# Kernel optimization log

Measured on AMD Instinct MI355X. Metric: run time of the kernel, lower is better.

Reference implementation:

```python
import jax, jax.numpy as jnp
import numpy as np

N = 50000      # nodes
E = 800000     # edges
IN = 128       # in_dim
EMB = 32       # emb_dim
ED = 8         # edge_dim
L = 4          # num_layers
B = 64         # num graphs in batch
OUT = 10       # out_dim
EPS = 1e-5


def setup_inputs() -> dict:
    key = jax.random.key(0)
    ks = jax.random.split(key, 16)
    f32 = jnp.float32
    def nrm(k, shape, scale):
        return jax.random.normal(k, shape, dtype=f32) * scale
    inp = {}
    inp['x'] = nrm(ks[0], (N, IN), 1.0)
    inp['edge_index'] = jax.random.randint(ks[1], (2, E), 0, N)
    inp['edge_attr'] = nrm(ks[2], (E, ED), 1.0)
    inp['batch'] = jnp.sort(jax.random.randint(ks[3], (N,), 0, B))
    # lin_in
    inp['lin_in_w'] = nrm(ks[4], (IN, EMB), 0.05)
    inp['lin_in_b'] = jnp.zeros((EMB,), f32)
    # per-layer message MLP: Linear(2e+ed->e), BN, ReLU, Linear(e->e), BN, ReLU
    inp['msg_w1'] = nrm(ks[5], (L, 2 * EMB + ED, EMB), 0.1)
    inp['msg_b1'] = jnp.zeros((L, EMB), f32)
    inp['msg_g1'] = jnp.ones((L, EMB), f32)
    inp['msg_be1'] = jnp.zeros((L, EMB), f32)
    inp['msg_w2'] = nrm(ks[6], (L, EMB, EMB), 0.1)
    inp['msg_b2'] = jnp.zeros((L, EMB), f32)
    inp['msg_g2'] = jnp.ones((L, EMB), f32)
    inp['msg_be2'] = jnp.zeros((L, EMB), f32)
    # per-layer update MLP: Linear(2e->e), BN, ReLU, Linear(e->e), BN, ReLU
    inp['upd_w1'] = nrm(ks[7], (L, 2 * EMB, EMB), 0.1)
    inp['upd_b1'] = jnp.zeros((L, EMB), f32)
    inp['upd_g1'] = jnp.ones((L, EMB), f32)
    inp['upd_be1'] = jnp.zeros((L, EMB), f32)
    inp['upd_w2'] = nrm(ks[8], (L, EMB, EMB), 0.1)
    inp['upd_b2'] = jnp.zeros((L, EMB), f32)
    inp['upd_g2'] = jnp.ones((L, EMB), f32)
    inp['upd_be2'] = jnp.zeros((L, EMB), f32)
    # lin_pred
    inp['pred_w'] = nrm(ks[9], (EMB, OUT), 0.1)
    inp['pred_b'] = jnp.zeros((OUT,), f32)
    return inp


def _bn(x, g, b):
    # BatchNorm1d in training mode: batch stats over dim 0 (biased variance)
    mu = jnp.mean(x, axis=0)
    var = jnp.mean(jnp.square(x - mu), axis=0)
    return (x - mu) * jax.lax.rsqrt(var + EPS) * g + b


def reference(x, edge_attr, lin_in_w, lin_in_b,
              msg_w1, msg_b1, msg_g1, msg_be1, msg_w2, msg_b2, msg_g2, msg_be2,
              upd_w1, upd_b1, upd_g1, upd_be1, upd_w2, upd_b2, upd_g2, upd_be2,
              pred_w, pred_b, edge_index, batch):
    src = edge_index[0]  # h_j source nodes
    dst = edge_index[1]  # h_i target nodes (aggregation index)
    h = x @ lin_in_w + lin_in_b  # [N, EMB]
    for i in range(L):
        # message: gather + concat + MLP(BN,ReLU)x2 over edges
        msg_in = jnp.concatenate([h[dst], h[src], edge_attr], axis=-1)  # [E, 2e+ed]
        m = jax.nn.relu(_bn(msg_in @ msg_w1[i] + msg_b1[i], msg_g1[i], msg_be1[i]))
        m = jax.nn.relu(_bn(m @ msg_w2[i] + msg_b2[i], msg_g2[i], msg_be2[i]))
        # aggregate: scatter-add by destination
        aggr = jax.ops.segment_sum(m, dst, num_segments=N)  # [N, EMB]
        # update: concat + MLP(BN,ReLU)x2
        u = jnp.concatenate([h, aggr], axis=-1)  # [N, 2e]
        u = jax.nn.relu(_bn(u @ upd_w1[i] + upd_b1[i], upd_g1[i], upd_be1[i]))
        u = jax.nn.relu(_bn(u @ upd_w2[i] + upd_b2[i], upd_g2[i], upd_be2[i]))
        h = u + h  # residual in MPNNModel.get_embeddings
    # global mean pool
    sums = jax.ops.segment_sum(h, batch, num_segments=B)
    counts = jax.ops.segment_sum(jnp.ones((N,), h.dtype), batch, num_segments=B)
    h_graph = sums / jnp.maximum(counts, 1.0)[:, None]
    return h_graph @ pred_w + pred_b  # [B, OUT]
```

## Files before the change

### kernel.cpp

```cpp
#include <hip/hip_runtime.h>
#include <cstddef>

#define N_NODES 50000
#define N_EDGES 800000
#define IN_DIM  128
#define EMB     32
#define ED      8
#define NLAYERS 4
#define NB      64
#define OUTD    10
#define EPS_BN  1e-5f

#define EDGE_GRID 3125
#define NODE_GRID 196
#define NODE4_GRID 782
#define AGGR_GRID 6250
#define MSG1_EPT  2
#define MSG1_GRID 1563
#define NT16      50000
#define MSG2_TPW  16
#define MSG2_GRID 782

#define SREP 4

typedef short bf16x8 __attribute__((ext_vector_type(8)));
typedef float f32x4  __attribute__((ext_vector_type(4)));


__device__ __forceinline__ unsigned short f2bf(float x) {
  union { float f; unsigned u; } v; v.f = x;
  unsigned b = v.u + 0x7FFFu + ((v.u >> 16) & 1u);
  return (unsigned short)(b >> 16);
}
__device__ __forceinline__ float bf2f(unsigned short s) {
  union { unsigned u; float f; } v; v.u = ((unsigned)s) << 16;
  return v.f;
}

__device__ __forceinline__ uint4 pack8_bf16(const float v[8]) {
  uint4 o;
  o.x = (unsigned)f2bf(v[0]) | ((unsigned)f2bf(v[1]) << 16);
  o.y = (unsigned)f2bf(v[2]) | ((unsigned)f2bf(v[3]) << 16);
  o.z = (unsigned)f2bf(v[4]) | ((unsigned)f2bf(v[5]) << 16);
  o.w = (unsigned)f2bf(v[6]) | ((unsigned)f2bf(v[7]) << 16);
  return o;
}

__device__ __forceinline__ void mac8_f4(float acc[8], const float4 v, const float* __restrict__ wk) {
#pragma unroll
  for (int j = 0; j < 8; ++j) acc[j] = fmaf(v.x, wk[j], acc[j]);
#pragma unroll
  for (int j = 0; j < 8; ++j) acc[j] = fmaf(v.y, wk[EMB + j], acc[j]);
#pragma unroll
  for (int j = 0; j < 8; ++j) acc[j] = fmaf(v.z, wk[2*EMB + j], acc[j]);
#pragma unroll
  for (int j = 0; j < 8; ++j) acc[j] = fmaf(v.w, wk[3*EMB + j], acc[j]);
}

__device__ __forceinline__ void coef_from_stats(const float* __restrict__ stats_stage,
                                                const float* __restrict__ g,
                                                const float* __restrict__ be,
                                                float inv_count, float* __restrict__ cf) {
  if (threadIdx.x < EMB) {
    const int c = threadIdx.x;
    float s = 0.f, ss = 0.f;
#pragma unroll
    for (int r = 0; r < SREP; ++r) {
      s  += stats_stage[r*64 + c];
      ss += stats_stage[r*64 + EMB + c];
    }
    const float mu  = s * inv_count;
    const float var = ss * inv_count - mu*mu;
    const float a = g[c] * rsqrtf(var + EPS_BN);
    cf[c] = a;
    cf[EMB + c] = fmaf(-mu, a, be[c]);
  }
  __syncthreads();
}

__device__ __forceinline__ void wave_stats_atomic(float ts[8], float tss[8],
                                                  float* __restrict__ lds_s,
                                                  float* __restrict__ lds_q,
                                                  float* __restrict__ stats_stage) {
  const int lane = threadIdx.x & 63;
  const int wv   = threadIdx.x >> 6;
#pragma unroll
  for (int j = 0; j < 8; ++j) {
    float a = ts[j], b = tss[j];
#pragma unroll
    for (int o = 32; o > 0; o >>= 1) {
      a += __shfl_down(a, o, 64);
      b += __shfl_down(b, o, 64);
    }
    ts[j] = a; tss[j] = b;
  }
  if (lane == 0) {
#pragma unroll
    for (int j = 0; j < 8; ++j) {
      lds_s[wv*8 + j] = ts[j];
      lds_q[wv*8 + j] = tss[j];
    }
  }
  __syncthreads();
  if (threadIdx.x < 64) {
    const float v = (threadIdx.x < 32) ? lds_s[threadIdx.x] : lds_q[threadIdx.x - 32];
    atomicAdd(stats_stage + ((blockIdx.x & (SREP-1)) << 6) + threadIdx.x, v);
  }
}

__device__ __forceinline__ void block_stats_atomic(const float ts[EMB], const float tss[EMB],
                                                   float* __restrict__ stats_stage) {
  __shared__ float sred[256];
  const int lane = threadIdx.x & 63;
  const int wid  = threadIdx.x >> 6;
#pragma unroll
  for (int c = 0; c < EMB; ++c) {
    float a = ts[c];
    float q = tss[c];
#pragma unroll
    for (int o = 32; o > 0; o >>= 1) {
      a += __shfl_down(a, o, 64);
      q += __shfl_down(q, o, 64);
    }
    if (lane == 0) { sred[wid*64 + c] = a; sred[wid*64 + EMB + c] = q; }
  }
  __syncthreads();
  if (threadIdx.x < 64) {
    const float v = sred[threadIdx.x] + sred[64 + threadIdx.x] +
                    sred[128 + threadIdx.x] + sred[192 + threadIdx.x];
    atomicAdd(stats_stage + ((blockIdx.x & (SREP-1)) << 6) + threadIdx.x, v);
  }
}


__global__ __launch_bounds__(256) void k_lin_in_pq(
    const float* __restrict__ x, const float* __restrict__ w, const float* __restrict__ b,
    const float* __restrict__ w1, const float* __restrict__ b1,
    float* __restrict__ h, unsigned short* __restrict__ p, unsigned short* __restrict__ q)
{
  __shared__ float lds_h[64][33];
  const int lane = threadIdx.x & 63;
  const int wv   = threadIdx.x >> 6;
  const int n  = blockIdx.x*64 + lane;
  const int c0 = wv*8;
  if (n < N_NODES) {
    float acc[8];
#pragma unroll
    for (int j = 0; j < 8; ++j) acc[j] = b[c0 + j];
    const float4* xp = (const float4*)(x + (size_t)n*IN_DIM);
#pragma unroll 8
    for (int k4 = 0; k4 < IN_DIM/4; ++k4)
      mac8_f4(acc, xp[k4], w + (k4*4)*EMB + c0);
    float4 o0, o1;
    o0.x = acc[0]; o0.y = acc[1]; o0.z = acc[2]; o0.w = acc[3];
    o1.x = acc[4]; o1.y = acc[5]; o1.z = acc[6]; o1.w = acc[7];
    *(float4*)(h + (size_t)n*EMB + c0)     = o0;
    *(float4*)(h + (size_t)n*EMB + c0 + 4) = o1;
#pragma unroll
    for (int j = 0; j < 8; ++j) lds_h[lane][c0 + j] = acc[j];
  }
  __syncthreads();
  if (n < N_NODES) {
    float ap[8], aq[8];
#pragma unroll
    for (int j = 0; j < 8; ++j) { ap[j] = b1[c0 + j]; aq[j] = 0.f; }
#pragma unroll
    for (int k = 0; k < EMB; ++k) {
      const float hv = lds_h[lane][k];
      const float* wp = w1 + k*EMB + c0;
      const float* wq = w1 + (EMB + k)*EMB + c0;
#pragma unroll
      for (int j = 0; j < 8; ++j) ap[j] = fmaf(hv, wp[j], ap[j]);
#pragma unroll
      for (int j = 0; j < 8; ++j) aq[j] = fmaf(hv, wq[j], aq[j]);
    }
    *(uint4*)(p + (size_t)n*EMB + c0) = pack8_bf16(ap);
    *(uint4*)(q + (size_t)n*EMB + c0) = pack8_bf16(aq);
  }
}

__global__ __launch_bounds__(256) void k_upd1(
    const float* __restrict__ h, float* __restrict__ aggr,
    const float* __restrict__ w, const float* __restrict__ b,
    float* __restrict__ stats)
{
  __shared__ float lds_s[32], lds_q[32];
  const int lane = threadIdx.x & 63;
  const int wv   = threadIdx.x >> 6;
  const int n  = blockIdx.x*64 + lane;
  const int c0 = wv*8;
  float acc[8];
#pragma unroll
  for (int j = 0; j < 8; ++j) acc[j] = 0.f;
  if (n < N_NODES) {
#pragma unroll
    for (int j = 0; j < 8; ++j) acc[j] = b[c0 + j];
    const float4* hp = (const float4*)(h + (size_t)n*EMB);
    const float4* ap = (const float4*)(aggr + (size_t)n*EMB);
#pragma unroll
    for (int k4 = 0; k4 < 8; ++k4) mac8_f4(acc, hp[k4], w + (k4*4)*EMB + c0);
#pragma unroll
    for (int k4 = 0; k4 < 8; ++k4) mac8_f4(acc, ap[k4], w + (EMB + k4*4)*EMB + c0);
  }
  float ts[8], tss[8];
#pragma unroll
  for (int j = 0; j < 8; ++j) { ts[j] = acc[j]; tss[j] = acc[j]*acc[j]; }
  wave_stats_atomic(ts, tss, lds_s, lds_q, stats);
  if (n < N_NODES) {
    float4 o0, o1;
    o0.x = acc[0]; o0.y = acc[1]; o0.z = acc[2]; o0.w = acc[3];
    o1.x = acc[4]; o1.y = acc[5]; o1.z = acc[6]; o1.w = acc[7];
    *(float4*)(aggr + (size_t)n*EMB + c0)     = o0;
    *(float4*)(aggr + (size_t)n*EMB + c0 + 4) = o1;
  }
}

__global__ __launch_bounds__(256) void k_upd2(
    float* __restrict__ z,
    const float* __restrict__ stats1, const float* __restrict__ g1, const float* __restrict__ be1,
    const float* __restrict__ w, const float* __restrict__ b,
    float* __restrict__ stats2)
{
  __shared__ float cf[64];
  __shared__ float lds_s[32], lds_q[32];
  coef_from_stats(stats1, g1, be1, 1.0f/(float)N_NODES, cf);

  const int lane = threadIdx.x & 63;
  const int wv   = threadIdx.x >> 6;
  const int n  = blockIdx.x*64 + lane;
  const int c0 = wv*8;
  float acc[8];
#pragma unroll
  for (int j = 0; j < 8; ++j) acc[j] = 0.f;
  if (n < N_NODES) {
#pragma unroll
    for (int j = 0; j < 8; ++j) acc[j] = b[c0 + j];
    const float4* zp = (const float4*)(z + (size_t)n*EMB);
#pragma unroll
    for (int k4 = 0; k4 < 8; ++k4) {
      const float4 v = zp[k4];
      const float mv[4] = {v.x, v.y, v.z, v.w};
#pragma unroll
      for (int t = 0; t < 4; ++t) {
        const int k = 4*k4 + t;
        const float m = fmaxf(fmaf(cf[k], mv[t], cf[EMB + k]), 0.f);
        const float* wk = w + k*EMB + c0;
#pragma unroll
        for (int j = 0; j < 8; ++j) acc[j] = fmaf(m, wk[j], acc[j]);
      }
    }
  }
  float ts[8], tss[8];
#pragma unroll
  for (int j = 0; j < 8; ++j) { ts[j] = acc[j]; tss[j] = acc[j]*acc[j]; }
  wave_stats_atomic(ts, tss, lds_s, lds_q, stats2);
  if (n < N_NODES) {
    float4 o0, o1;
    o0.x = acc[0]; o0.y = acc[1]; o0.z = acc[2]; o0.w = acc[3];
    o1.x = acc[4]; o1.y = acc[5]; o1.z = acc[6]; o1.w = acc[7];
    *(float4*)(z + (size_t)n*EMB + c0)     = o0;
    *(float4*)(z + (size_t)n*EMB + c0 + 4) = o1;
  }
}

__global__ __launch_bounds__(256) void k_resid_pq(
    float* __restrict__ h, const float* __restrict__ z,
    const float* __restrict__ stats, const float* __restrict__ g, const float* __restrict__ be,
    const float* __restrict__ w1_next, const float* __restrict__ b1_next,
    unsigned short* __restrict__ p, unsigned short* __restrict__ q)
{
  __shared__ float cf[64];
  __shared__ float lds_h[64][33];
  coef_from_stats(stats, g, be, 1.0f/(float)N_NODES, cf);

  const int lane = threadIdx.x & 63;
  const int wv   = threadIdx.x >> 6;
  const int n  = blockIdx.x*64 + lane;
  const int c0 = wv*8;
  if (n < N_NODES) {
    const float4* zp = (const float4*)(z + (size_t)n*EMB + c0);
    float4* hp = (float4*)(h + (size_t)n*EMB + c0);
    float hn[8];
    const float4 z0 = zp[0], z1 = zp[1];
    const float4 h0 = hp[0], h1 = hp[1];
    const float zv[8] = {z0.x, z0.y, z0.z, z0.w, z1.x, z1.y, z1.z, z1.w};
    const float hv[8] = {h0.x, h0.y, h0.z, h0.w, h1.x, h1.y, h1.z, h1.w};
#pragma unroll
    for (int j = 0; j < 8; ++j) {
      const int k = c0 + j;
      hn[j] = hv[j] + fmaxf(fmaf(cf[k], zv[j], cf[EMB + k]), 0.f);
      lds_h[lane][k] = hn[j];
    }
    float4 o0, o1;
    o0.x = hn[0]; o0.y = hn[1]; o0.z = hn[2]; o0.w = hn[3];
    o1.x = hn[4]; o1.y = hn[5]; o1.z = hn[6]; o1.w = hn[7];
    hp[0] = o0; hp[1] = o1;
  }
  __syncthreads();
  if (n < N_NODES && w1_next) {
    float ap[8], aq[8];
#pragma unroll
    for (int j = 0; j < 8; ++j) { ap[j] = b1_next[c0 + j]; aq[j] = 0.f; }
#pragma unroll
    for (int k = 0; k < EMB; ++k) {
      const float hvv = lds_h[lane][k];
      const float* wp = w1_next + k*EMB + c0;
      const float* wq = w1_next + (EMB + k)*EMB + c0;
#pragma unroll
      for (int j = 0; j < 8; ++j) ap[j] = fmaf(hvv, wp[j], ap[j]);
#pragma unroll
      for (int j = 0; j < 8; ++j) aq[j] = fmaf(hvv, wq[j], aq[j]);
    }
    *(uint4*)(p + (size_t)n*EMB + c0) = pack8_bf16(ap);
    *(uint4*)(q + (size_t)n*EMB + c0) = pack8_bf16(aq);
  }
}

__global__ __launch_bounds__(256) void k_hist(const int* __restrict__ ei, int* __restrict__ cnt) {
  const int e = blockIdx.x*256 + threadIdx.x;
  if (e < N_EDGES) atomicAdd(&cnt[ei[N_EDGES + e]], 1);
}

__global__ __launch_bounds__(256) void k_scan_a(const int* __restrict__ cnt,
                                                int* __restrict__ row_ptr, int* __restrict__ bsum) {
  __shared__ int s[256];
  const int gid = blockIdx.x*256 + threadIdx.x;
  const int v = (gid < N_NODES) ? cnt[gid] : 0;
  s[threadIdx.x] = v;
  __syncthreads();
  for (int o = 1; o < 256; o <<= 1) {
    const int t = (threadIdx.x >= o) ? s[threadIdx.x - o] : 0;
    __syncthreads();
    s[threadIdx.x] += t;
    __syncthreads();
  }
  if (gid < N_NODES) row_ptr[gid] = s[threadIdx.x] - v;
  if (threadIdx.x == 255) bsum[blockIdx.x] = s[255];
}

__global__ __launch_bounds__(256) void k_scan_b(int* __restrict__ bsum, int* __restrict__ row_ptr) {
  __shared__ int s[256];
  const int v = (threadIdx.x < NODE_GRID) ? bsum[threadIdx.x] : 0;
  s[threadIdx.x] = v;
  __syncthreads();
  for (int o = 1; o < 256; o <<= 1) {
    const int t = (threadIdx.x >= o) ? s[threadIdx.x - o] : 0;
    __syncthreads();
    s[threadIdx.x] += t;
    __syncthreads();
  }
  if (threadIdx.x < NODE_GRID) bsum[threadIdx.x] = s[threadIdx.x] - v;
  if (threadIdx.x == 0) row_ptr[N_NODES] = N_EDGES;
}

__global__ __launch_bounds__(256) void k_scan_c(int* __restrict__ row_ptr, const int* __restrict__ bsum) {
  const int gid = blockIdx.x*256 + threadIdx.x;
  if (gid < N_NODES) row_ptr[gid] += bsum[blockIdx.x];
}

__global__ __launch_bounds__(256) void k_place(const int* __restrict__ ei,
                                               const int* __restrict__ row_ptr,
                                               int* __restrict__ cnt2, int* __restrict__ perm) {
  const int e = blockIdx.x*256 + threadIdx.x;
  if (e >= N_EDGES) return;
  const int d = ei[N_EDGES + e];
  const int pos = row_ptr[d] + atomicAdd(&cnt2[d], 1);
  perm[pos] = e;
}

__global__ __launch_bounds__(256) void k_permute(
    const int* __restrict__ perm, const int* __restrict__ ei, const float* __restrict__ ea,
    int* __restrict__ src_perm, int* __restrict__ dst_perm, unsigned short* __restrict__ ea_perm)
{
  const int i = blockIdx.x*256 + threadIdx.x;
  const int e = perm[i];
  src_perm[i] = ei[e];
  dst_perm[i] = ei[N_EDGES + e];
  const float4* src4 = (const float4*)(ea + (size_t)e*ED);
  const float4 v0 = src4[0], v1 = src4[1];
  const float ev[8] = {v0.x, v0.y, v0.z, v0.w, v1.x, v1.y, v1.z, v1.w};
  unsigned u[4];
#pragma unroll
  for (int j = 0; j < 4; ++j)
    u[j] = (unsigned)f2bf(ev[2*j]) | ((unsigned)f2bf(ev[2*j+1]) << 16);
  uint4 o; o.x = u[0]; o.y = u[1]; o.z = u[2]; o.w = u[3];
  *(uint4*)(ea_perm + (size_t)i*ED) = o;
}


__global__ __launch_bounds__(256) void k_msg1(
    const unsigned short* __restrict__ pb, const unsigned short* __restrict__ qb,
    const int* __restrict__ src_perm, const int* __restrict__ dst_perm,
    const unsigned short* __restrict__ ea_perm,
    const float* __restrict__ w1b,
    unsigned short* __restrict__ y, float* __restrict__ stats)
{
  float ts[EMB], tss[EMB];
#pragma unroll
  for (int c = 0; c < EMB; ++c) { ts[c] = 0.f; tss[c] = 0.f; }
  const int base = blockIdx.x*(256*MSG1_EPT) + threadIdx.x;
  for (int it = 0; it < MSG1_EPT; ++it) {
    const int i = base + it*256;
    if (i >= N_EDGES) break;
    const int dst = dst_perm[i];
    const int src = src_perm[i];
    float acc[EMB];
    const uint4* pd = (const uint4*)(pb + (size_t)dst*EMB);
    const uint4* qs = (const uint4*)(qb + (size_t)src*EMB);
#pragma unroll
    for (int j4 = 0; j4 < 4; ++j4) {
      const uint4 a = pd[j4];
      const uint4 b = qs[j4];
      const unsigned ua[4] = {a.x, a.y, a.z, a.w};
      const unsigned ub[4] = {b.x, b.y, b.z, b.w};
#pragma unroll
      for (int t = 0; t < 4; ++t) {
        acc[j4*8 + 2*t]   = bf2f((unsigned short)(ua[t] & 0xFFFFu)) +
                            bf2f((unsigned short)(ub[t] & 0xFFFFu));
        acc[j4*8 + 2*t+1] = bf2f((unsigned short)(ua[t] >> 16)) +
                            bf2f((unsigned short)(ub[t] >> 16));
      }
    }
    const uint4 eraw = *(const uint4*)(ea_perm + (size_t)i*ED);
    const unsigned ue[4] = {eraw.x, eraw.y, eraw.z, eraw.w};
    float ev[8];
#pragma unroll
    for (int t = 0; t < 4; ++t) {
      ev[2*t]   = bf2f((unsigned short)(ue[t] & 0xFFFFu));
      ev[2*t+1] = bf2f((unsigned short)(ue[t] >> 16));
    }
#pragma unroll
    for (int k = 0; k < 8; ++k) {
      const float* wk = w1b + k*EMB;
#pragma unroll
      for (int c = 0; c < EMB; ++c) acc[c] = fmaf(ev[k], wk[c], acc[c]);
    }

    unsigned short us[EMB];
#pragma unroll
    for (int c = 0; c < EMB; ++c) us[c] = f2bf(acc[c]);
    unsigned u[16];
#pragma unroll
    for (int j = 0; j < 16; ++j)
      u[j] = (unsigned)us[2*j] | ((unsigned)us[2*j+1] << 16);
    uint4* dp = (uint4*)(y + (size_t)i*EMB);
#pragma unroll
    for (int j = 0; j < 4; ++j) {
      uint4 o; o.x = u[4*j]; o.y = u[4*j+1]; o.z = u[4*j+2]; o.w = u[4*j+3];
      dp[j] = o;
    }
#pragma unroll
    for (int c = 0; c < EMB; ++c) {
      const float v = bf2f(us[c]);
      ts[c] += v;
      tss[c] = fmaf(v, v, tss[c]);
    }
  }
  block_stats_atomic(ts, tss, stats);
}

__global__ __launch_bounds__(256) void k_msg2(
    unsigned short* __restrict__ y,
    const float* __restrict__ stats1, const float* __restrict__ g1, const float* __restrict__ be1,
    const float* __restrict__ w2, const float* __restrict__ b2,
    float* __restrict__ stats2)
{
  __shared__ __align__(16) unsigned short lds_t[4][16*32];
  __shared__ float lds_s[4][32], lds_q[4][32];
  __shared__ float cf[64];

  coef_from_stats(stats1, g1, be1, 1.0f/(float)N_EDGES, cf);

  const int lane = threadIdx.x & 63;
  const int wid  = threadIdx.x >> 6;
  const int n0 = lane & 15;
  const int kb = lane >> 4;

  bf16x8 Blo, Bhi;
#pragma unroll
  for (int j = 0; j < 8; ++j) {
    Blo[j] = (short)f2bf(w2[(kb*8 + j)*EMB + n0]);
    Bhi[j] = (short)f2bf(w2[(kb*8 + j)*EMB + 16 + n0]);
  }
  float a1[8], c1[8];
#pragma unroll
  for (int j = 0; j < 8; ++j) {
    a1[j] = cf[kb*8 + j];
    c1[j] = cf[EMB + kb*8 + j];
  }
  const float b2c0 = b2[n0], b2c1 = b2[16 + n0];

  float ts[8], tss[8];
#pragma unroll
  for (int j = 0; j < 8; ++j) { ts[j] = 0.f; tss[j] = 0.f; }

  const int tile0 = blockIdx.x * (MSG2_TPW*4);
  for (int t = 0; t < MSG2_TPW; ++t) {
    const int tile = tile0 + t*4 + wid;
    if (tile >= NT16) break;
    const size_t e0 = (size_t)tile * 16;

    const uint4 araw = *(const uint4*)(y + (e0 + n0)*EMB + kb*8);
    unsigned int ua[4] = {araw.x, araw.y, araw.z, araw.w};
    bf16x8 A;
#pragma unroll
    for (int j = 0; j < 4; ++j) {
      float v0 = bf2f((unsigned short)(ua[j] & 0xFFFFu));
      float v1 = bf2f((unsigned short)(ua[j] >> 16));
      v0 = fmaxf(fmaf(a1[2*j],   v0, c1[2*j]),   0.f);
      v1 = fmaxf(fmaf(a1[2*j+1], v1, c1[2*j+1]), 0.f);
      A[2*j]   = (short)f2bf(v0);
      A[2*j+1] = (short)f2bf(v1);
    }

    f32x4 acc0 = {0.f, 0.f, 0.f, 0.f};
    f32x4 acc1 = {0.f, 0.f, 0.f, 0.f};
    acc0 = __builtin_amdgcn_mfma_f32_16x16x32_bf16(A, Blo, acc0, 0, 0, 0);
    acc1 = __builtin_amdgcn_mfma_f32_16x16x32_bf16(A, Bhi, acc1, 0, 0, 0);

#pragma unroll
    for (int r = 0; r < 4; ++r) {
      const int row = kb*4 + r;
      lds_t[wid][row*32 + n0]      = f2bf(acc0[r] + b2c0);
      lds_t[wid][row*32 + 16 + n0] = f2bf(acc1[r] + b2c1);
    }
    const uint4 orow = *(const uint4*)&lds_t[wid][(lane>>2)*32 + (lane&3)*8];
    *(uint4*)(y + (e0 + (lane>>2))*EMB + (lane&3)*8) = orow;

    unsigned int uo[4] = {orow.x, orow.y, orow.z, orow.w};
#pragma unroll
    for (int j = 0; j < 4; ++j) {
      const float v0 = bf2f((unsigned short)(uo[j] & 0xFFFFu));
      const float v1 = bf2f((unsigned short)(uo[j] >> 16));
      ts[2*j]   += v0;  tss[2*j]   = fmaf(v0, v0, tss[2*j]);
      ts[2*j+1] += v1;  tss[2*j+1] = fmaf(v1, v1, tss[2*j+1]);
    }
  }

#pragma unroll
  for (int j = 0; j < 8; ++j) {
    float s = ts[j], qq = tss[j];
#pragma unroll
    for (int o = 4; o < 64; o <<= 1) {
      s  += __shfl_xor(s, o, 64);
      qq += __shfl_xor(qq, o, 64);
    }
    ts[j] = s; tss[j] = qq;
  }
  if (lane < 4) {
#pragma unroll
    for (int j = 0; j < 8; ++j) {
      lds_s[wid][lane*8 + j] = ts[j];
      lds_q[wid][lane*8 + j] = tss[j];
    }
  }
  __syncthreads();
  if (threadIdx.x < 64) {
    const int c = threadIdx.x & 31;
    const int kind = threadIdx.x >> 5;
    float v = 0.f;
#pragma unroll
    for (int wq = 0; wq < 4; ++wq)
      v += kind ? lds_q[wq][c] : lds_s[wq][c];
    atomicAdd(stats2 + ((blockIdx.x & (SREP-1)) << 6) + kind*32 + c, v);
  }
}

__global__ __launch_bounds__(256) void k_aggr(
    const unsigned short* __restrict__ y, const int* __restrict__ row_ptr,
    const float* __restrict__ stats2, const float* __restrict__ g2, const float* __restrict__ be2,
    float* __restrict__ aggr)
{
  __shared__ float cf[64];
  coef_from_stats(stats2, g2, be2, 1.0f/(float)N_EDGES, cf);

  const int grp = threadIdx.x >> 5;
  const int l   = threadIdx.x & 31;
  const int rof = l >> 4;
  const int cp  = l & 15;
  const int n = blockIdx.x*8 + grp;
  if (n >= N_NODES) return;
  const float a0 = cf[2*cp],     b0 = cf[EMB + 2*cp];
  const float a1 = cf[2*cp + 1], b1 = cf[EMB + 2*cp + 1];
  const int lo = row_ptr[n], hi = row_ptr[n+1];
  float s0 = 0.f, s1 = 0.f;
  for (int i = lo + rof; i < hi; i += 2) {
    const unsigned u = *(const unsigned*)(y + (size_t)i*EMB + 2*cp);
    const float v0 = bf2f((unsigned short)(u & 0xFFFFu));
    const float v1 = bf2f((unsigned short)(u >> 16));
    s0 += fmaxf(fmaf(a0, v0, b0), 0.f);
    s1 += fmaxf(fmaf(a1, v1, b1), 0.f);
  }
  s0 += __shfl_xor(s0, 16, 64);
  s1 += __shfl_xor(s1, 16, 64);
  if (rof == 0) {
    float2 o; o.x = s0; o.y = s1;
    *(float2*)(aggr + (size_t)n*EMB + 2*cp) = o;
  }
}

__global__ void k_pool(const float* __restrict__ h, const int* __restrict__ batch,
                       const float* __restrict__ pw, const float* __restrict__ pb,
                       float* __restrict__ out)
{
  __shared__ float sred[256];
  __shared__ float hg[EMB];
  const int b = blockIdx.x;
  int lo = 0, hi = N_NODES;
  while (lo < hi) { int m = (lo + hi) >> 1; if (batch[m] < b) lo = m + 1; else hi = m; }
  const int start = lo;
  hi = N_NODES;
  while (lo < hi) { int m = (lo + hi) >> 1; if (batch[m] < b + 1) lo = m + 1; else hi = m; }
  const int end = lo;

  const int c = threadIdx.x & (EMB-1);
  const int r = threadIdx.x >> 5;
  float s = 0.f;
  for (int n = start + r; n < end; n += 8) s += h[(size_t)n*EMB + c];
  sred[threadIdx.x] = s;
  __syncthreads();
  if (threadIdx.x < EMB) {
    float tot = 0.f;
#pragma unroll
    for (int r2 = 0; r2 < 8; ++r2) tot += sred[r2*EMB + threadIdx.x];
    const float cnt = (float)(end - start);
    hg[threadIdx.x] = tot / fmaxf(cnt, 1.f);
  }
  __syncthreads();
  if (threadIdx.x < OUTD) {
    float acc = pb[threadIdx.x];
#pragma unroll
    for (int cc = 0; cc < EMB; ++cc) acc = fmaf(hg[cc], pw[cc*OUTD + threadIdx.x], acc);
    out[b*OUTD + threadIdx.x] = acc;
  }
}


extern "C" void kernel_launch(void* const* d_in, const int* in_sizes, int n_in,
                              void* d_out, int out_size, void* d_ws, size_t ws_size,
                              hipStream_t stream) {
  const float* x        = (const float*)d_in[0];
  const int*   ei       = (const int*)  d_in[1];
  const float* ea       = (const float*)d_in[2];
  const int*   batch    = (const int*)  d_in[3];
  const float* lin_in_w = (const float*)d_in[4];
  const float* lin_in_b = (const float*)d_in[5];
  const float* msg_w1   = (const float*)d_in[6];
  const float* msg_b1   = (const float*)d_in[7];
  const float* msg_g1   = (const float*)d_in[8];
  const float* msg_be1  = (const float*)d_in[9];
  const float* msg_w2   = (const float*)d_in[10];
  const float* msg_b2   = (const float*)d_in[11];
  const float* msg_g2   = (const float*)d_in[12];
  const float* msg_be2  = (const float*)d_in[13];
  const float* upd_w1   = (const float*)d_in[14];
  const float* upd_b1   = (const float*)d_in[15];
  const float* upd_g1   = (const float*)d_in[16];
  const float* upd_be1  = (const float*)d_in[17];
  const float* upd_w2   = (const float*)d_in[18];
  const float* upd_b2   = (const float*)d_in[19];
  const float* upd_g2   = (const float*)d_in[20];
  const float* upd_be2  = (const float*)d_in[21];
  const float* pred_w   = (const float*)d_in[22];
  const float* pred_b   = (const float*)d_in[23];
  float* out = (float*)d_out;

  char* wsb = (char*)d_ws;
  unsigned short* y  = (unsigned short*)wsb;
  unsigned short* eap= (unsigned short*)(wsb + (size_t)N_EDGES*EMB*2);
  unsigned short* p  = eap + (size_t)N_EDGES*ED;
  unsigned short* q  = p + (size_t)N_NODES*EMB;
  float* h       = (float*)(q + (size_t)N_NODES*EMB);
  float* aggr    = h + (size_t)N_NODES*EMB;
  float* stats   = aggr + (size_t)N_NODES*EMB;
  int*   cnt     = (int*)(stats + 16*SREP*64);
  int*   cnt2    = cnt + N_NODES;
  int*   row_ptr = cnt2 + N_NODES;
  int*   bsum    = row_ptr + N_NODES + 1;
  int*   perm    = bsum + 256;
  int*   src_perm= perm + N_EDGES;
  int*   dst_perm= src_perm + N_EDGES;
  const size_t need = ((size_t)((char*)(dst_perm + N_EDGES) - wsb));
  if (ws_size < need) return;

  hipMemsetAsync(stats, 0, (16*SREP*64 + 2*N_NODES)*sizeof(float), stream);

  k_lin_in_pq<<<NODE4_GRID, 256, 0, stream>>>(x, lin_in_w, lin_in_b, msg_w1, msg_b1, h, p, q);
  k_hist<<<EDGE_GRID, 256, 0, stream>>>(ei, cnt);
  k_scan_a<<<NODE_GRID, 256, 0, stream>>>(cnt, row_ptr, bsum);
  k_scan_b<<<1, 256, 0, stream>>>(bsum, row_ptr);
  k_scan_c<<<NODE_GRID, 256, 0, stream>>>(row_ptr, bsum);
  k_place<<<EDGE_GRID, 256, 0, stream>>>(ei, row_ptr, cnt2, perm);
  k_permute<<<EDGE_GRID, 256, 0, stream>>>(perm, ei, ea, src_perm, dst_perm, eap);

  for (int l = 0; l < NLAYERS; ++l) {
    const int st = l*4;
    const float* w1  = msg_w1 + (size_t)l*(2*EMB+ED)*EMB;
    const float* w1b = w1 + (size_t)2*EMB*EMB;
    const float* w2  = msg_w2 + (size_t)l*EMB*EMB;
    const float* uw1 = upd_w1 + (size_t)l*(2*EMB)*EMB;
    const float* uw2 = upd_w2 + (size_t)l*EMB*EMB;
    const float* w1_next = (l+1 < NLAYERS) ? msg_w1 + (size_t)(l+1)*(2*EMB+ED)*EMB : nullptr;
    const float* b1_next = (l+1 < NLAYERS) ? msg_b1 + (size_t)(l+1)*EMB : nullptr;

    k_msg1<<<MSG1_GRID, 256, 0, stream>>>(p, q, src_perm, dst_perm, eap,
                                          w1b, y, stats + (size_t)st*SREP*64);
    k_msg2<<<MSG2_GRID, 256, 0, stream>>>(y, stats + (size_t)st*SREP*64,
                                          msg_g1 + l*EMB, msg_be1 + l*EMB,
                                          w2, msg_b2 + l*EMB, stats + (size_t)(st+1)*SREP*64);
    k_aggr<<<AGGR_GRID, 256, 0, stream>>>(y, row_ptr, stats + (size_t)(st+1)*SREP*64,
                                          msg_g2 + l*EMB, msg_be2 + l*EMB, aggr);
    k_upd1<<<NODE4_GRID, 256, 0, stream>>>(h, aggr, uw1, upd_b1 + l*EMB,
                                           stats + (size_t)(st+2)*SREP*64);
    k_upd2<<<NODE4_GRID, 256, 0, stream>>>(aggr, stats + (size_t)(st+2)*SREP*64,
                                           upd_g1 + l*EMB, upd_be1 + l*EMB,
                                           uw2, upd_b2 + l*EMB, stats + (size_t)(st+3)*SREP*64);
    k_resid_pq<<<NODE4_GRID, 256, 0, stream>>>(h, aggr, stats + (size_t)(st+3)*SREP*64,
                                               upd_g2 + l*EMB, upd_be2 + l*EMB,
                                               w1_next, b1_next, p, q);
  }

  k_pool<<<NB, 256, 0, stream>>>(h, batch, pred_w, pred_b, out);
}
```

Before: 951.7 us.

## Fuse all GNN stages into one persistent cooperative kernel with grid syncs

Replaces about thirty separate kernel launches (preprocessing, four layers of six stages each, and pooling) with a single cooperative persistent kernel that loops over work with grid-stride loops and separates dependent stages with grid.sync(). The goal is to remove per-launch overhead and the gaps between dependent kernels. In exchange the grid is capped at occupancy × 256 CUs (at most 1024 blocks), register pressure rises from merging every stage into one kernel, and each stage now pays a grid-wide barrier. A new z buffer is added to the workspace.

```diff
diff --git a/kernel.cpp b/kernel.cpp
--- a/kernel.cpp
+++ b/kernel.cpp
@@ -1,5 +1,8 @@
 #include <hip/hip_runtime.h>
+#include <hip/hip_cooperative_groups.h>
 #include <cstddef>
+
+namespace cg = cooperative_groups;
 
 #define N_NODES 50000
 #define N_EDGES 800000
@@ -11,16 +14,8 @@
 #define OUTD    10
 #define EPS_BN  1e-5f
 
-#define EDGE_GRID 3125
 #define NODE_GRID 196
-#define NODE4_GRID 782
-#define AGGR_GRID 6250
-#define MSG1_EPT  2
-#define MSG1_GRID 1563
 #define NT16      50000
-#define MSG2_TPW  16
-#define MSG2_GRID 782
-
 #define SREP 4
 
 typedef short bf16x8 __attribute__((ext_vector_type(8)));
@@ -46,7 +41,7 @@
   return o;
 }
 
-__device__ __forceinline__ void mac8_f4(float acc[8], const float4 v, const float* __restrict__ wk) {
+__device__ __forceinline__ void mac8_f4(float acc[8], const float4 v, const float* wk) {
 #pragma unroll
   for (int j = 0; j < 8; ++j) acc[j] = fmaf(v.x, wk[j], acc[j]);
 #pragma unroll
@@ -57,581 +52,583 @@
   for (int j = 0; j < 8; ++j) acc[j] = fmaf(v.w, wk[3*EMB + j], acc[j]);
 }
 
-__device__ __forceinline__ void coef_from_stats(const float* __restrict__ stats_stage,
-                                                const float* __restrict__ g,
-                                                const float* __restrict__ be,
-                                                float inv_count, float* __restrict__ cf) {
-  if (threadIdx.x < EMB) {
-    const int c = threadIdx.x;
-    float s = 0.f, ss = 0.f;
-#pragma unroll
-    for (int r = 0; r < SREP; ++r) {
-      s  += stats_stage[r*64 + c];
-      ss += stats_stage[r*64 + EMB + c];
-    }
-    const float mu  = s * inv_count;
-    const float var = ss * inv_count - mu*mu;
-    const float a = g[c] * rsqrtf(var + EPS_BN);
-    cf[c] = a;
-    cf[EMB + c] = fmaf(-mu, a, be[c]);
+struct KArgs {
+  const float* x; const int* ei; const float* ea; const int* batch;
+  const float *lin_in_w, *lin_in_b;
+  const float *msg_w1, *msg_b1, *msg_g1, *msg_be1;
+  const float *msg_w2, *msg_b2, *msg_g2, *msg_be2;
+  const float *upd_w1, *upd_b1, *upd_g1, *upd_be1;
+  const float *upd_w2, *upd_b2, *upd_g2, *upd_be2;
+  const float *pred_w, *pred_b;
+  unsigned short *y, *eap, *p, *q;
+  float *h, *aggr, *z, *stats;
+  int *cnt, *cnt2, *row_ptr, *bsum, *perm, *src_perm, *dst_perm;
+  float* out;
+};
+
+
+__global__ __launch_bounds__(256, 4) void k_all(KArgs a)
+{
+  cg::grid_group grid = cg::this_grid();
+  const int tid  = threadIdx.x;
+  const int lane = tid & 63;
+  const int wv   = tid >> 6;
+  const int nblk = gridDim.x;
+
+  __shared__ float lds_h[64][33];
+  __shared__ __align__(16) unsigned short lds_t[4][512];
+  __shared__ float lds_s4[4][32], lds_q4[4][32];
+  __shared__ float lds_ws_s[32], lds_ws_q[32];
+  __shared__ float sred[256];
+  __shared__ float cf[64];
+  __shared__ int   sscan[256];
+  __shared__ float hg[EMB];
+
+  const float invE = 1.0f / (float)N_EDGES;
+  const float invN = 1.0f / (float)N_NODES;
+
+  for (int n0 = blockIdx.x*64; n0 < N_NODES; n0 += nblk*64) {
+    const int n  = n0 + lane;
+    const int c0 = wv*8;
+    if (n < N_NODES) {
+      float acc[8];
+#pragma unroll
+      for (int j = 0; j < 8; ++j) acc[j] = a.lin_in_b[c0 + j];
+      const float4* xp = (const float4*)(a.x + (size_t)n*IN_DIM);
+#pragma unroll 8
+      for (int k4 = 0; k4 < IN_DIM/4; ++k4)
+        mac8_f4(acc, xp[k4], a.lin_in_w + (k4*4)*EMB + c0);
+      float4 o0, o1;
+      o0.x = acc[0]; o0.y = acc[1]; o0.z = acc[2]; o0.w = acc[3];
+      o1.x = acc[4]; o1.y = acc[5]; o1.z = acc[6]; o1.w = acc[7];
+      *(float4*)(a.h + (size_t)n*EMB + c0)     = o0;
+      *(float4*)(a.h + (size_t)n*EMB + c0 + 4) = o1;
+#pragma unroll
+      for (int j = 0; j < 8; ++j) lds_h[lane][c0 + j] = acc[j];
+    }
+    __syncthreads();
+    if (n < N_NODES) {
+      float ap[8], aq[8];
+#pragma unroll
+      for (int j = 0; j < 8; ++j) { ap[j] = a.msg_b1[c0 + j]; aq[j] = 0.f; }
+#pragma unroll
+      for (int k = 0; k < EMB; ++k) {
+        const float hv = lds_h[lane][k];
+        const float* wp = a.msg_w1 + k*EMB + c0;
+        const float* wq = a.msg_w1 + (EMB + k)*EMB + c0;
+#pragma unroll
+        for (int j = 0; j < 8; ++j) ap[j] = fmaf(hv, wp[j], ap[j]);
+#pragma unroll
+        for (int j = 0; j < 8; ++j) aq[j] = fmaf(hv, wq[j], aq[j]);
+      }
+      *(uint4*)(a.p + (size_t)n*EMB + c0) = pack8_bf16(ap);
+      *(uint4*)(a.q + (size_t)n*EMB + c0) = pack8_bf16(aq);
+    }
+    __syncthreads();
   }
-  __syncthreads();
-}
-
-__device__ __forceinline__ void wave_stats_atomic(float ts[8], float tss[8],
-                                                  float* __restrict__ lds_s,
-                                                  float* __restrict__ lds_q,
-                                                  float* __restrict__ stats_stage) {
-  const int lane = threadIdx.x & 63;
-  const int wv   = threadIdx.x >> 6;
-#pragma unroll
-  for (int j = 0; j < 8; ++j) {
-    float a = ts[j], b = tss[j];
-#pragma unroll
-    for (int o = 32; o > 0; o >>= 1) {
-      a += __shfl_down(a, o, 64);
-      b += __shfl_down(b, o, 64);
-    }
-    ts[j] = a; tss[j] = b;
+  for (int e = blockIdx.x*256 + tid; e < N_EDGES; e += nblk*256)
+    atomicAdd(&a.cnt[a.ei[N_EDGES + e]], 1);
+  grid.sync();
+
+  for (int blk = blockIdx.x; blk < NODE_GRID; blk += nblk) {
+    const int gid = blk*256 + tid;
+    const int v = (gid < N_NODES) ? a.cnt[gid] : 0;
+    sscan[tid] = v;
+    __syncthreads();
+    for (int o = 1; o < 256; o <<= 1) {
+      const int t = (tid >= o) ? sscan[tid - o] : 0;
+      __syncthreads();
+      sscan[tid] += t;
+      __syncthreads();
+    }
+    if (gid < N_NODES) a.row_ptr[gid] = sscan[tid] - v;
+    if (tid == 255) a.bsum[blk] = sscan[255];
+    __syncthreads();
   }
-  if (lane == 0) {
-#pragma unroll
-    for (int j = 0; j < 8; ++j) {
-      lds_s[wv*8 + j] = ts[j];
-      lds_q[wv*8 + j] = tss[j];
-    }
+  grid.sync();
+
+  if (blockIdx.x == 0) {
+    const int v = (tid < NODE_GRID) ? a.bsum[tid] : 0;
+    sscan[tid] = v;
+    __syncthreads();
+    for (int o = 1; o < 256; o <<= 1) {
+      const int t = (tid >= o) ? sscan[tid - o] : 0;
+      __syncthreads();
+      sscan[tid] += t;
+      __syncthreads();
+    }
+    if (tid < NODE_GRID) a.bsum[tid] = sscan[tid] - v;
+    if (tid == 0) a.row_ptr[N_NODES] = N_EDGES;
   }
-  __syncthreads();
-  if (threadIdx.x < 64) {
-    const float v = (threadIdx.x < 32) ? lds_s[threadIdx.x] : lds_q[threadIdx.x - 32];
-    atomicAdd(stats_stage + ((blockIdx.x & (SREP-1)) << 6) + threadIdx.x, v);
+  grid.sync();
+
+  for (int gid = blockIdx.x*256 + tid; gid < N_NODES; gid += nblk*256)
+    a.row_ptr[gid] += a.bsum[gid >> 8];
+  grid.sync();
+
+  for (int e = blockIdx.x*256 + tid; e < N_EDGES; e += nblk*256) {
+    const int d = a.ei[N_EDGES + e];
+    const int pos = a.row_ptr[d] + atomicAdd(&a.cnt2[d], 1);
+    a.perm[pos] = e;
   }
-}
-
-__device__ __forceinline__ void block_stats_atomic(const float ts[EMB], const float tss[EMB],
-                                                   float* __restrict__ stats_stage) {
-  __shared__ float sred[256];
-  const int lane = threadIdx.x & 63;
-  const int wid  = threadIdx.x >> 6;
-#pragma unroll
-  for (int c = 0; c < EMB; ++c) {
-    float a = ts[c];
-    float q = tss[c];
-#pragma unroll
-    for (int o = 32; o > 0; o >>= 1) {
-      a += __shfl_down(a, o, 64);
-      q += __shfl_down(q, o, 64);
-    }
-    if (lane == 0) { sred[wid*64 + c] = a; sred[wid*64 + EMB + c] = q; }
+  grid.sync();
+
+  for (int i = blockIdx.x*256 + tid; i < N_EDGES; i += nblk*256) {
+    const int e = a.perm[i];
+    a.src_perm[i] = a.ei[e];
+    a.dst_perm[i] = a.ei[N_EDGES + e];
+    const float4* src4 = (const float4*)(a.ea + (size_t)e*ED);
+    const float4 v0 = src4[0], v1 = src4[1];
+    const float ev[8] = {v0.x, v0.y, v0.z, v0.w, v1.x, v1.y, v1.z, v1.w};
+    unsigned u[4];
+#pragma unroll
+    for (int j = 0; j < 4; ++j)
+      u[j] = (unsigned)f2bf(ev[2*j]) | ((unsigned)f2bf(ev[2*j+1]) << 16);
+    uint4 o; o.x = u[0]; o.y = u[1]; o.z = u[2]; o.w = u[3];
+    *(uint4*)(a.eap + (size_t)i*ED) = o;
   }
-  __syncthreads();
-  if (threadIdx.x < 64) {
-    const float v = sred[threadIdx.x] + sred[64 + threadIdx.x] +
-                    sred[128 + threadIdx.x] + sred[192 + threadIdx.x];
-    atomicAdd(stats_stage + ((blockIdx.x & (SREP-1)) << 6) + threadIdx.x, v);
+  grid.sync();
+
+  for (int l = 0; l < NLAYERS; ++l) {
+    const int st = l*4;
+    const float* w1b = a.msg_w1 + (size_t)l*(2*EMB+ED)*EMB + (size_t)2*EMB*EMB;
+    const float* w2  = a.msg_w2 + (size_t)l*EMB*EMB;
+    const float* uw1 = a.upd_w1 + (size_t)l*(2*EMB)*EMB;
+    const float* uw2 = a.upd_w2 + (size_t)l*EMB*EMB;
+    float* st0 = a.stats + (size_t)st*SREP*64;
+    float* st1 = a.stats + (size_t)(st+1)*SREP*64;
+    float* st2 = a.stats + (size_t)(st+2)*SREP*64;
+    float* st3 = a.stats + (size_t)(st+3)*SREP*64;
+
+    {
+      float ts[EMB], tss[EMB];
+#pragma unroll
+      for (int c = 0; c < EMB; ++c) { ts[c] = 0.f; tss[c] = 0.f; }
+      for (int i = blockIdx.x*256 + tid; i < N_EDGES; i += nblk*256) {
+        const int dst = a.dst_perm[i];
+        const int src = a.src_perm[i];
+        float acc[EMB];
+        const uint4* pd = (const uint4*)(a.p + (size_t)dst*EMB);
+        const uint4* qs = (const uint4*)(a.q + (size_t)src*EMB);
+#pragma unroll
+        for (int j4 = 0; j4 < 4; ++j4) {
+          const uint4 av = pd[j4];
+          const uint4 bv = qs[j4];
+          const unsigned ua[4] = {av.x, av.y, av.z, av.w};
+          const unsigned ub[4] = {bv.x, bv.y, bv.z, bv.w};
+#pragma unroll
+          for (int t = 0; t < 4; ++t) {
+            acc[j4*8 + 2*t]   = bf2f((unsigned short)(ua[t] & 0xFFFFu)) +
+                                bf2f((unsigned short)(ub[t] & 0xFFFFu));
+            acc[j4*8 + 2*t+1] = bf2f((unsigned short)(ua[t] >> 16)) +
+                                bf2f((unsigned short)(ub[t] >> 16));
+          }
+        }
+        const uint4 eraw = *(const uint4*)(a.eap + (size_t)i*ED);
+        const unsigned ue[4] = {eraw.x, eraw.y, eraw.z, eraw.w};
+        float ev[8];
+#pragma unroll
+        for (int t = 0; t < 4; ++t) {
+          ev[2*t]   = bf2f((unsigned short)(ue[t] & 0xFFFFu));
+          ev[2*t+1] = bf2f((unsigned short)(ue[t] >> 16));
+        }
+#pragma unroll
+        for (int k = 0; k < 8; ++k) {
+          const float* wk = w1b + k*EMB;
+#pragma unroll
+          for (int c = 0; c < EMB; ++c) acc[c] = fmaf(ev[k], wk[c], acc[c]);
+        }
+        unsigned short us[EMB];
+#pragma unroll
+        for (int c = 0; c < EMB; ++c) us[c] = f2bf(acc[c]);
+        unsigned u[16];
+#pragma unroll
+        for (int j = 0; j < 16; ++j)
+          u[j] = (unsigned)us[2*j] | ((unsigned)us[2*j+1] << 16);
+        uint4* dp = (uint4*)(a.y + (size_t)i*EMB);
+#pragma unroll
+        for (int j = 0; j < 4; ++j) {
+          uint4 o; o.x = u[4*j]; o.y = u[4*j+1]; o.z = u[4*j+2]; o.w = u[4*j+3];
+          dp[j] = o;
+        }
+#pragma unroll
+        for (int c = 0; c < EMB; ++c) {
+          const float v = bf2f(us[c]);
+          ts[c] += v;
+          tss[c] = fmaf(v, v, tss[c]);
+        }
+      }
+#pragma unroll
+      for (int c = 0; c < EMB; ++c) {
+        float aa = ts[c];
+        float qq = tss[c];
+#pragma unroll
+        for (int o = 32; o > 0; o >>= 1) {
+          aa += __shfl_down(aa, o, 64);
+          qq += __shfl_down(qq, o, 64);
+        }
+        if (lane == 0) { sred[wv*64 + c] = aa; sred[wv*64 + EMB + c] = qq; }
+      }
+      __syncthreads();
+      if (tid < 64) {
+        const float v = sred[tid] + sred[64 + tid] + sred[128 + tid] + sred[192 + tid];
+        atomicAdd(st0 + ((blockIdx.x & (SREP-1)) << 6) + tid, v);
+      }
+      __syncthreads();
+    }
+    grid.sync();
+
+    {
+      if (tid < EMB) {
+        float s = 0.f, ss = 0.f;
+#pragma unroll
+        for (int r = 0; r < SREP; ++r) { s += st0[r*64 + tid]; ss += st0[r*64 + EMB + tid]; }
+        const float mu  = s * invE;
+        const float var = ss * invE - mu*mu;
+        const float aa = a.msg_g1[l*EMB + tid] * rsqrtf(var + EPS_BN);
+        cf[tid] = aa;
+        cf[EMB + tid] = fmaf(-mu, aa, a.msg_be1[l*EMB + tid]);
+      }
+      __syncthreads();
+
+      const int n0i = lane & 15;
+      const int kb  = lane >> 4;
+      bf16x8 Blo, Bhi;
+#pragma unroll
+      for (int j = 0; j < 8; ++j) {
+        Blo[j] = (short)f2bf(w2[(kb*8 + j)*EMB + n0i]);
+        Bhi[j] = (short)f2bf(w2[(kb*8 + j)*EMB + 16 + n0i]);
+      }
+      float a1[8], c1[8];
+#pragma unroll
+      for (int j = 0; j < 8; ++j) {
+        a1[j] = cf[kb*8 + j];
+        c1[j] = cf[EMB + kb*8 + j];
+      }
+      const float b2c0 = a.msg_b2[l*EMB + n0i], b2c1 = a.msg_b2[l*EMB + 16 + n0i];
+
+      float ts8[8], tss8[8];
+#pragma unroll
+      for (int j = 0; j < 8; ++j) { ts8[j] = 0.f; tss8[j] = 0.f; }
+
+      for (int tile = blockIdx.x*4 + wv; tile < NT16; tile += nblk*4) {
+        const size_t e0 = (size_t)tile * 16;
+        const uint4 araw = *(const uint4*)(a.y + (e0 + n0i)*EMB + kb*8);
+        unsigned int ua[4] = {araw.x, araw.y, araw.z, araw.w};
+        bf16x8 A;
+#pragma unroll
+        for (int j = 0; j < 4; ++j) {
+          float v0 = bf2f((unsigned short)(ua[j] & 0xFFFFu));
+          float v1 = bf2f((unsigned short)(ua[j] >> 16));
+          v0 = fmaxf(fmaf(a1[2*j],   v0, c1[2*j]),   0.f);
+          v1 = fmaxf(fmaf(a1[2*j+1], v1, c1[2*j+1]), 0.f);
+          A[2*j]   = (short)f2bf(v0);
+          A[2*j+1] = (short)f2bf(v1);
+        }
+        f32x4 acc0 = {0.f, 0.f, 0.f, 0.f};
+        f32x4 acc1 = {0.f, 0.f, 0.f, 0.f};
+        acc0 = __builtin_amdgcn_mfma_f32_16x16x32_bf16(A, Blo, acc0, 0, 0, 0);
+        acc1 = __builtin_amdgcn_mfma_f32_16x16x32_bf16(A, Bhi, acc1, 0, 0, 0);
+#pragma unroll
+        for (int r = 0; r < 4; ++r) {
+          const int row = kb*4 + r;
+          lds_t[wv][row*32 + n0i]      = f2bf(acc0[r] + b2c0);
+          lds_t[wv][row*32 + 16 + n0i] = f2bf(acc1[r] + b2c1);
+        }
+        const uint4 orow = *(const uint4*)&lds_t[wv][(lane>>2)*32 + (lane&3)*8];
+        *(uint4*)(a.y + (e0 + (lane>>2))*EMB + (lane&3)*8) = orow;
+        unsigned int uo[4] = {orow.x, orow.y, orow.z, orow.w};
+#pragma unroll
+        for (int j = 0; j < 4; ++j) {
+          const float v0 = bf2f((unsigned short)(uo[j] & 0xFFFFu));
+          const float v1 = bf2f((unsigned short)(uo[j] >> 16));
+          ts8[2*j]   += v0;  tss8[2*j]   = fmaf(v0, v0, tss8[2*j]);
+          ts8[2*j+1] += v1;  tss8[2*j+1] = fmaf(v1, v1, tss8[2*j+1]);
+        }
+      }
+#pragma unroll
+      for (int j = 0; j < 8; ++j) {
+        float s = ts8[j], qq = tss8[j];
+#pragma unroll
+        for (int o = 4; o < 64; o <<= 1) {
+          s  += __shfl_xor(s, o, 64);
+          qq += __shfl_xor(qq, o, 64);
+        }
+        ts8[j] = s; tss8[j] = qq;
+      }
+      if (lane < 4) {
+#pragma unroll
+        for (int j = 0; j < 8; ++j) {
+          lds_s4[wv][lane*8 + j] = ts8[j];
+          lds_q4[wv][lane*8 + j] = tss8[j];
+        }
+      }
+      __syncthreads();
+      if (tid < 64) {
+        const int c = tid & 31;
+        const int kind = tid >> 5;
+        float v = 0.f;
+#pragma unroll
+        for (int wq = 0; wq < 4; ++wq)
+          v += kind ? lds_q4[wq][c] : lds_s4[wq][c];
+        atomicAdd(st1 + ((blockIdx.x & (SREP-1)) << 6) + kind*32 + c, v);
+      }
+      __syncthreads();
+    }
+    grid.sync();
+
+    {
+      if (tid < EMB) {
+        float s = 0.f, ss = 0.f;
+#pragma unroll
+        for (int r = 0; r < SREP; ++r) { s += st1[r*64 + tid]; ss += st1[r*64 + EMB + tid]; }
+        const float mu  = s * invE;
+        const float var = ss * invE - mu*mu;
+        const float aa = a.msg_g2[l*EMB + tid] * rsqrtf(var + EPS_BN);
+        cf[tid] = aa;
+        cf[EMB + tid] = fmaf(-mu, aa, a.msg_be2[l*EMB + tid]);
+      }
+      __syncthreads();
+
+      const int grp = tid >> 5;
+      const int ll  = tid & 31;
+      const int rof = ll >> 4;
+      const int cp  = ll & 15;
+      const float a0 = cf[2*cp],     b0 = cf[EMB + 2*cp];
+      const float a1c = cf[2*cp + 1], b1c = cf[EMB + 2*cp + 1];
+      for (int n = blockIdx.x*8 + grp; n < N_NODES; n += nblk*8) {
+        const int lo = a.row_ptr[n], hi = a.row_ptr[n+1];
+        float s0 = 0.f, s1 = 0.f;
+        for (int i = lo + rof; i < hi; i += 2) {
+          const unsigned u = *(const unsigned*)(a.y + (size_t)i*EMB + 2*cp);
+          const float v0 = bf2f((unsigned short)(u & 0xFFFFu));
+          const float v1 = bf2f((unsigned short)(u >> 16));
+          s0 += fmaxf(fmaf(a0, v0, b0), 0.f);
+          s1 += fmaxf(fmaf(a1c, v1, b1c), 0.f);
+        }
+        s0 += __shfl_xor(s0, 16, 64);
+        s1 += __shfl_xor(s1, 16, 64);
+        if (rof == 0) {
+          float2 o; o.x = s0; o.y = s1;
+          *(float2*)(a.aggr + (size_t)n*EMB + 2*cp) = o;
+        }
+      }
+      __syncthreads();
+    }
+    grid.sync();
+
+    {
+      const int c0 = wv*8;
+      float ts8[8], tss8[8];
+#pragma unroll
+      for (int j = 0; j < 8; ++j) { ts8[j] = 0.f; tss8[j] = 0.f; }
+      for (int nb0 = blockIdx.x*64; nb0 < N_NODES; nb0 += nblk*64) {
+        const int n = nb0 + lane;
+        float acc[8];
+#pragma unroll
+        for (int j = 0; j < 8; ++j) acc[j] = 0.f;
+        if (n < N_NODES) {
+#pragma unroll
+          for (int j = 0; j < 8; ++j) acc[j] = a.upd_b1[l*EMB + c0 + j];
+          const float4* hp = (const float4*)(a.h + (size_t)n*EMB);
+          const float4* ap = (const float4*)(a.aggr + (size_t)n*EMB);
+#pragma unroll
+          for (int k4 = 0; k4 < 8; ++k4) mac8_f4(acc, hp[k4], uw1 + (k4*4)*EMB + c0);
+#pragma unroll
+          for (int k4 = 0; k4 < 8; ++k4) mac8_f4(acc, ap[k4], uw1 + (EMB + k4*4)*EMB + c0);
+          float4 o0, o1;
+          o0.x = acc[0]; o0.y = acc[1]; o0.z = acc[2]; o0.w = acc[3];
+          o1.x = acc[4]; o1.y = acc[5]; o1.z = acc[6]; o1.w = acc[7];
+          *(float4*)(a.z + (size_t)n*EMB + c0)     = o0;
+          *(float4*)(a.z + (size_t)n*EMB + c0 + 4) = o1;
+        }
+#pragma unroll
+        for (int j = 0; j < 8; ++j) { ts8[j] += acc[j]; tss8[j] = fmaf(acc[j], acc[j], tss8[j]); }
+      }
+#pragma unroll
+      for (int j = 0; j < 8; ++j) {
+        float aa = ts8[j], bb = tss8[j];
+#pragma unroll
+        for (int o = 32; o > 0; o >>= 1) {
+          aa += __shfl_down(aa, o, 64);
+          bb += __shfl_down(bb, o, 64);
+        }
+        ts8[j] = aa; tss8[j] = bb;
+      }
+      if (lane == 0) {
+#pragma unroll
+        for (int j = 0; j < 8; ++j) { lds_ws_s[wv*8 + j] = ts8[j]; lds_ws_q[wv*8 + j] = tss8[j]; }
+      }
+      __syncthreads();
+      if (tid < 64) {
+        const float v = (tid < 32) ? lds_ws_s[tid] : lds_ws_q[tid - 32];
+        atomicAdd(st2 + ((blockIdx.x & (SREP-1)) << 6) + tid, v);
+      }
+      __syncthreads();
+    }
+    grid.sync();
+
+    {
+      if (tid < EMB) {
+        float s = 0.f, ss = 0.f;
+#pragma unroll
+        for (int r = 0; r < SREP; ++r) { s += st2[r*64 + tid]; ss += st2[r*64 + EMB + tid]; }
+        const float mu  = s * invN;
+        const float var = ss * invN - mu*mu;
+        const float aa = a.upd_g1[l*EMB + tid] * rsqrtf(var + EPS_BN);
+        cf[tid] = aa;
+        cf[EMB + tid] = fmaf(-mu, aa, a.upd_be1[l*EMB + tid]);
+      }
+      __syncthreads();
+
+      const int c0 = wv*8;
+      float ts8[8], tss8[8];
+#pragma unroll
+      for (int j = 0; j < 8; ++j) { ts8[j] = 0.f; tss8[j] = 0.f; }
+      for (int nb0 = blockIdx.x*64; nb0 < N_NODES; nb0 += nblk*64) {
+        const int n = nb0 + lane;
+        float acc[8];
+#pragma unroll
+        for (int j = 0; j < 8; ++j) acc[j] = 0.f;
+        if (n < N_NODES) {
+#pragma unroll
+          for (int j = 0; j < 8; ++j) acc[j] = a.upd_b2[l*EMB + c0 + j];
+          const float4* zp = (const float4*)(a.z + (size_t)n*EMB);
+#pragma unroll
+          for (int k4 = 0; k4 < 8; ++k4) {
+            const float4 v = zp[k4];
+            const float mv[4] = {v.x, v.y, v.z, v.w};
+#pragma unroll
+            for (int t = 0; t < 4; ++t) {
+              const int k = 4*k4 + t;
+              const float m = fmaxf(fmaf(cf[k], mv[t], cf[EMB + k]), 0.f);
+              const float* wk = uw2 + k*EMB + c0;
+#pragma unroll
+              for (int j = 0; j < 8; ++j) acc[j] = fmaf(m, wk[j], acc[j]);
+            }
+          }
+          float4 o0, o1;
+          o0.x = acc[0]; o0.y = acc[1]; o0.z = acc[2]; o0.w = acc[3];
+          o1.x = acc[4]; o1.y = acc[5]; o1.z = acc[6]; o1.w = acc[7];
+          *(float4*)(a.aggr + (size_t)n*EMB + c0)     = o0;
+          *(float4*)(a.aggr + (size_t)n*EMB + c0 + 4) = o1;
+        }
+#pragma unroll
+        for (int j = 0; j < 8; ++j) { ts8[j] += acc[j]; tss8[j] = fmaf(acc[j], acc[j], tss8[j]); }
+      }
+#pragma unroll
+      for (int j = 0; j < 8; ++j) {
+        float aa = ts8[j], bb = tss8[j];
+#pragma unroll
+        for (int o = 32; o > 0; o >>= 1) {
+          aa += __shfl_down(aa, o, 64);
+          bb += __shfl_down(bb, o, 64);
+        }
+        ts8[j] = aa; tss8[j] = bb;
+      }
+      if (lane == 0) {
+#pragma unroll
+        for (int j = 0; j < 8; ++j) { lds_ws_s[wv*8 + j] = ts8[j]; lds_ws_q[wv*8 + j] = tss8[j]; }
+      }
+      __syncthreads();
+      if (tid < 64) {
+        const float v = (tid < 32) ? lds_ws_s[tid] : lds_ws_q[tid - 32];
+        atomicAdd(st3 + ((blockIdx.x & (SREP-1)) << 6) + tid, v);
+      }
+      __syncthreads();
+    }
+    grid.sync();
+
+    {
+      if (tid < EMB) {
+        float s = 0.f, ss = 0.f;
+#pragma unroll
+        for (int r = 0; r < SREP; ++r) { s += st3[r*64 + tid]; ss += st3[r*64 + EMB + tid]; }
+        const float mu  = s * invN;
+        const float var = ss * invN - mu*mu;
+        const float aa = a.upd_g2[l*EMB + tid] * rsqrtf(var + EPS_BN);
+        cf[tid] = aa;
+        cf[EMB + tid] = fmaf(-mu, aa, a.upd_be2[l*EMB + tid]);
+      }
+      __syncthreads();
+
+      const float* w1n = (l+1 < NLAYERS) ? a.msg_w1 + (size_t)(l+1)*(2*EMB+ED)*EMB : nullptr;
+      const float* b1n = (l+1 < NLAYERS) ? a.msg_b1 + (size_t)(l+1)*EMB : nullptr;
+      const int c0 = wv*8;
+      for (int nb0 = blockIdx.x*64; nb0 < N_NODES; nb0 += nblk*64) {
+        const int n = nb0 + lane;
+        if (n < N_NODES) {
+          const float4* zp = (const float4*)(a.aggr + (size_t)n*EMB + c0);
+          float4* hp = (float4*)(a.h + (size_t)n*EMB + c0);
+          float hn[8];
+          const float4 z0 = zp[0], z1 = zp[1];
+          const float4 h0 = hp[0], h1 = hp[1];
+          const float zv[8] = {z0.x, z0.y, z0.z, z0.w, z1.x, z1.y, z1.z, z1.w};
+          const float hv[8] = {h0.x, h0.y, h0.z, h0.w, h1.x, h1.y, h1.z, h1.w};
+#pragma unroll
+          for (int j = 0; j < 8; ++j) {
+            const int k = c0 + j;
+            hn[j] = hv[j] + fmaxf(fmaf(cf[k], zv[j], cf[EMB + k]), 0.f);
+            lds_h[lane][k] = hn[j];
+          }
+          float4 o0, o1;
+          o0.x = hn[0]; o0.y = hn[1]; o0.z = hn[2]; o0.w = hn[3];
+          o1.x = hn[4]; o1.y = hn[5]; o1.z = hn[6]; o1.w = hn[7];
+          hp[0] = o0; hp[1] = o1;
+        }
+        __syncthreads();
+        if (n < N_NODES && w1n) {
+          float ap[8], aq[8];
+#pragma unroll
+          for (int j = 0; j < 8; ++j) { ap[j] = b1n[c0 + j]; aq[j] = 0.f; }
+#pragma unroll
+          for (int k = 0; k < EMB; ++k) {
+            const float hvv = lds_h[lane][k];
+            const float* wp = w1n + k*EMB + c0;
+            const float* wq = w1n + (EMB + k)*EMB + c0;
+#pragma unroll
+            for (int j = 0; j < 8; ++j) ap[j] = fmaf(hvv, wp[j], ap[j]);
+#pragma unroll
+            for (int j = 0; j < 8; ++j) aq[j] = fmaf(hvv, wq[j], aq[j]);
+          }
+          *(uint4*)(a.p + (size_t)n*EMB + c0) = pack8_bf16(ap);
+          *(uint4*)(a.q + (size_t)n*EMB + c0) = pack8_bf16(aq);
+        }
+        __syncthreads();
+      }
+    }
+    grid.sync();
   }
-}
-
-
-__global__ __launch_bounds__(256) void k_lin_in_pq(
-    const float* __restrict__ x, const float* __restrict__ w, const float* __restrict__ b,
-    const float* __restrict__ w1, const float* __restrict__ b1,
-    float* __restrict__ h, unsigned short* __restrict__ p, unsigned short* __restrict__ q)
-{
-  __shared__ float lds_h[64][33];
-  const int lane = threadIdx.x & 63;
-  const int wv   = threadIdx.x >> 6;
-  const int n  = blockIdx.x*64 + lane;
-  const int c0 = wv*8;
-  if (n < N_NODES) {
-    float acc[8];
-#pragma unroll
-    for (int j = 0; j < 8; ++j) acc[j] = b[c0 + j];
-    const float4* xp = (const float4*)(x + (size_t)n*IN_DIM);
-#pragma unroll 8
-    for (int k4 = 0; k4 < IN_DIM/4; ++k4)
-      mac8_f4(acc, xp[k4], w + (k4*4)*EMB + c0);
-    float4 o0, o1;
-    o0.x = acc[0]; o0.y = acc[1]; o0.z = acc[2]; o0.w = acc[3];
-    o1.x = acc[4]; o1.y = acc[5]; o1.z = acc[6]; o1.w = acc[7];
-    *(float4*)(h + (size_t)n*EMB + c0)     = o0;
-    *(float4*)(h + (size_t)n*EMB + c0 + 4) = o1;
-#pragma unroll
-    for (int j = 0; j < 8; ++j) lds_h[lane][c0 + j] = acc[j];
-  }
-  __syncthreads();
-  if (n < N_NODES) {
-    float ap[8], aq[8];
-#pragma unroll
-    for (int j = 0; j < 8; ++j) { ap[j] = b1[c0 + j]; aq[j] = 0.f; }
-#pragma unroll
-    for (int k = 0; k < EMB; ++k) {
-      const float hv = lds_h[lane][k];
-      const float* wp = w1 + k*EMB + c0;
-      const float* wq = w1 + (EMB + k)*EMB + c0;
-#pragma unroll
-      for (int j = 0; j < 8; ++j) ap[j] = fmaf(hv, wp[j], ap[j]);
-#pragma unroll
-      for (int j = 0; j < 8; ++j) aq[j] = fmaf(hv, wq[j], aq[j]);
-    }
-    *(uint4*)(p + (size_t)n*EMB + c0) = pack8_bf16(ap);
-    *(uint4*)(q + (size_t)n*EMB + c0) = pack8_bf16(aq);
-  }
-}
-
-__global__ __launch_bounds__(256) void k_upd1(
-    const float* __restrict__ h, float* __restrict__ aggr,
-    const float* __restrict__ w, const float* __restrict__ b,
-    float* __restrict__ stats)
-{
-  __shared__ float lds_s[32], lds_q[32];
-  const int lane = threadIdx.x & 63;
-  const int wv   = threadIdx.x >> 6;
-  const int n  = blockIdx.x*64 + lane;
-  const int c0 = wv*8;
-  float acc[8];
-#pragma unroll
-  for (int j = 0; j < 8; ++j) acc[j] = 0.f;
-  if (n < N_NODES) {
-#pragma unroll
-    for (int j = 0; j < 8; ++j) acc[j] = b[c0 + j];
-    const float4* hp = (const float4*)(h + (size_t)n*EMB);
-    const float4* ap = (const float4*)(aggr + (size_t)n*EMB);
-#pragma unroll
-    for (int k4 = 0; k4 < 8; ++k4) mac8_f4(acc, hp[k4], w + (k4*4)*EMB + c0);
-#pragma unroll
-    for (int k4 = 0; k4 < 8; ++k4) mac8_f4(acc, ap[k4], w + (EMB + k4*4)*EMB + c0);
-  }
-  float ts[8], tss[8];
-#pragma unroll
-  for (int j = 0; j < 8; ++j) { ts[j] = acc[j]; tss[j] = acc[j]*acc[j]; }
-  wave_stats_atomic(ts, tss, lds_s, lds_q, stats);
-  if (n < N_NODES) {
-    float4 o0, o1;
-    o0.x = acc[0]; o0.y = acc[1]; o0.z = acc[2]; o0.w = acc[3];
-    o1.x = acc[4]; o1.y = acc[5]; o1.z = acc[6]; o1.w = acc[7];
-    *(float4*)(aggr + (size_t)n*EMB + c0)     = o0;
-    *(float4*)(aggr + (size_t)n*EMB + c0 + 4) = o1;
-  }
-}
-
-__global__ __launch_bounds__(256) void k_upd2(
-    float* __restrict__ z,
-    const float* __restrict__ stats1, const float* __restrict__ g1, const float* __restrict__ be1,
-    const float* __restrict__ w, const float* __restrict__ b,
-    float* __restrict__ stats2)
-{
-  __shared__ float cf[64];
-  __shared__ float lds_s[32], lds_q[32];
-  coef_from_stats(stats1, g1, be1, 1.0f/(float)N_NODES, cf);
-
-  const int lane = threadIdx.x & 63;
-  const int wv   = threadIdx.x >> 6;
-  const int n  = blockIdx.x*64 + lane;
-  const int c0 = wv*8;
-  float acc[8];
-#pragma unroll
-  for (int j = 0; j < 8; ++j) acc[j] = 0.f;
-  if (n < N_NODES) {
-#pragma unroll
-    for (int j = 0; j < 8; ++j) acc[j] = b[c0 + j];
-    const float4* zp = (const float4*)(z + (size_t)n*EMB);
-#pragma unroll
-    for (int k4 = 0; k4 < 8; ++k4) {
-      const float4 v = zp[k4];
-      const float mv[4] = {v.x, v.y, v.z, v.w};
-#pragma unroll
-      for (int t = 0; t < 4; ++t) {
-        const int k = 4*k4 + t;
-        const float m = fmaxf(fmaf(cf[k], mv[t], cf[EMB + k]), 0.f);
-        const float* wk = w + k*EMB + c0;
-#pragma unroll
-        for (int j = 0; j < 8; ++j) acc[j] = fmaf(m, wk[j], acc[j]);
-      }
-    }
-  }
-  float ts[8], tss[8];
-#pragma unroll
-  for (int j = 0; j < 8; ++j) { ts[j] = acc[j]; tss[j] = acc[j]*acc[j]; }
-  wave_stats_atomic(ts, tss, lds_s, lds_q, stats2);
-  if (n < N_NODES) {
-    float4 o0, o1;
-    o0.x = acc[0]; o0.y = acc[1]; o0.z = acc[2]; o0.w = acc[3];
-    o1.x = acc[4]; o1.y = acc[5]; o1.z = acc[6]; o1.w = acc[7];
-    *(float4*)(z + (size_t)n*EMB + c0)     = o0;
-    *(float4*)(z + (size_t)n*EMB + c0 + 4) = o1;
-  }
-}
-
-__global__ __launch_bounds__(256) void k_resid_pq(
-    float* __restrict__ h, const float* __restrict__ z,
-    const float* __restrict__ stats, const float* __restrict__ g, const float* __restrict__ be,
-    const float* __restrict__ w1_next, const float* __restrict__ b1_next,
-    unsigned short* __restrict__ p, unsigned short* __restrict__ q)
-{
-  __shared__ float cf[64];
-  __shared__ float lds_h[64][33];
-  coef_from_stats(stats, g, be, 1.0f/(float)N_NODES, cf);
-
-  const int lane = threadIdx.x & 63;
-  const int wv   = threadIdx.x >> 6;
-  const int n  = blockIdx.x*64 + lane;
-  const int c0 = wv*8;
-  if (n < N_NODES) {
-    const float4* zp = (const float4*)(z + (size_t)n*EMB + c0);
-    float4* hp = (float4*)(h + (size_t)n*EMB + c0);
-    float hn[8];
-    const float4 z0 = zp[0], z1 = zp[1];
-    const float4 h0 = hp[0], h1 = hp[1];
-    const float zv[8] = {z0.x, z0.y, z0.z, z0.w, z1.x, z1.y, z1.z, z1.w};
-    const float hv[8] = {h0.x, h0.y, h0.z, h0.w, h1.x, h1.y, h1.z, h1.w};
-#pragma unroll
-    for (int j = 0; j < 8; ++j) {
-      const int k = c0 + j;
-      hn[j] = hv[j] + fmaxf(fmaf(cf[k], zv[j], cf[EMB + k]), 0.f);
-      lds_h[lane][k] = hn[j];
-    }
-    float4 o0, o1;
-    o0.x = hn[0]; o0.y = hn[1]; o0.z = hn[2]; o0.w = hn[3];
-    o1.x = hn[4]; o1.y = hn[5]; o1.z = hn[6]; o1.w = hn[7];
-    hp[0] = o0; hp[1] = o1;
-  }
-  __syncthreads();
-  if (n < N_NODES && w1_next) {
-    float ap[8], aq[8];
-#pragma unroll
-    for (int j = 0; j < 8; ++j) { ap[j] = b1_next[c0 + j]; aq[j] = 0.f; }
-#pragma unroll
-    for (int k = 0; k < EMB; ++k) {
-      const float hvv = lds_h[lane][k];
-      const float* wp = w1_next + k*EMB + c0;
-      const float* wq = w1_next + (EMB + k)*EMB + c0;
-#pragma unroll
-      for (int j = 0; j < 8; ++j) ap[j] = fmaf(hvv, wp[j], ap[j]);
-#pragma unroll
-      for (int j = 0; j < 8; ++j) aq[j] = fmaf(hvv, wq[j], aq[j]);
-    }
-    *(uint4*)(p + (size_t)n*EMB + c0) = pack8_bf16(ap);
-    *(uint4*)(q + (size_t)n*EMB + c0) = pack8_bf16(aq);
-  }
-}
-
-__global__ __launch_bounds__(256) void k_hist(const int* __restrict__ ei, int* __restrict__ cnt) {
-  const int e = blockIdx.x*256 + threadIdx.x;
-  if (e < N_EDGES) atomicAdd(&cnt[ei[N_EDGES + e]], 1);
-}
-
-__global__ __launch_bounds__(256) void k_scan_a(const int* __restrict__ cnt,
-                                                int* __restrict__ row_ptr, int* __restrict__ bsum) {
-  __shared__ int s[256];
-  const int gid = blockIdx.x*256 + threadIdx.x;
-  const int v = (gid < N_NODES) ? cnt[gid] : 0;
-  s[threadIdx.x] = v;
-  __syncthreads();
-  for (int o = 1; o < 256; o <<= 1) {
-    const int t = (threadIdx.x >= o) ? s[threadIdx.x - o] : 0;
-    __syncthreads();
-    s[threadIdx.x] += t;
-    __syncthreads();
-  }
-  if (gid < N_NODES) row_ptr[gid] = s[threadIdx.x] - v;
-  if (threadIdx.x == 255) bsum[blockIdx.x] = s[255];
-}
-
-__global__ __launch_bounds__(256) void k_scan_b(int* __restrict__ bsum, int* __restrict__ row_ptr) {
-  __shared__ int s[256];
-  const int v = (threadIdx.x < NODE_GRID) ? bsum[threadIdx.x] : 0;
-  s[threadIdx.x] = v;
-  __syncthreads();
-  for (int o = 1; o < 256; o <<= 1) {
-    const int t = (threadIdx.x >= o) ? s[threadIdx.x - o] : 0;
-    __syncthreads();
-    s[threadIdx.x] += t;
-    __syncthreads();
-  }
-  if (threadIdx.x < NODE_GRID) bsum[threadIdx.x] = s[threadIdx.x] - v;
-  if (threadIdx.x == 0) row_ptr[N_NODES] = N_EDGES;
-}
-
-__global__ __launch_bounds__(256) void k_scan_c(int* __restrict__ row_ptr, const int* __restrict__ bsum) {
-  const int gid = blockIdx.x*256 + threadIdx.x;
-  if (gid < N_NODES) row_ptr[gid] += bsum[blockIdx.x];
-}
-
-__global__ __launch_bounds__(256) void k_place(const int* __restrict__ ei,
-                                               const int* __restrict__ row_ptr,
-                                               int* __restrict__ cnt2, int* __restrict__ perm) {
-  const int e = blockIdx.x*256 + threadIdx.x;
-  if (e >= N_EDGES) return;
-  const int d = ei[N_EDGES + e];
-  const int pos = row_ptr[d] + atomicAdd(&cnt2[d], 1);
-  perm[pos] = e;
-}
-
-__global__ __launch_bounds__(256) void k_permute(
-    const int* __restrict__ perm, const int* __restrict__ ei, const float* __restrict__ ea,
-    int* __restrict__ src_perm, int* __restrict__ dst_perm, unsigned short* __restrict__ ea_perm)
-{
-  const int i = blockIdx.x*256 + threadIdx.x;
-  const int e = perm[i];
-  src_perm[i] = ei[e];
-  dst_perm[i] = ei[N_EDGES + e];
-  const float4* src4 = (const float4*)(ea + (size_t)e*ED);
-  const float4 v0 = src4[0], v1 = src4[1];
-  const float ev[8] = {v0.x, v0.y, v0.z, v0.w, v1.x, v1.y, v1.z, v1.w};
-  unsigned u[4];
-#pragma unroll
-  for (int j = 0; j < 4; ++j)
-    u[j] = (unsigned)f2bf(ev[2*j]) | ((unsigned)f2bf(ev[2*j+1]) << 16);
-  uint4 o; o.x = u[0]; o.y = u[1]; o.z = u[2]; o.w = u[3];
-  *(uint4*)(ea_perm + (size_t)i*ED) = o;
-}
-
-
-__global__ __launch_bounds__(256) void k_msg1(
-    const unsigned short* __restrict__ pb, const unsigned short* __restrict__ qb,
-    const int* __restrict__ src_perm, const int* __restrict__ dst_perm,
-    const unsigned short* __restrict__ ea_perm,
-    const float* __restrict__ w1b,
-    unsigned short* __restrict__ y, float* __restrict__ stats)
-{
-  float ts[EMB], tss[EMB];
-#pragma unroll
-  for (int c = 0; c < EMB; ++c) { ts[c] = 0.f; tss[c] = 0.f; }
-  const int base = blockIdx.x*(256*MSG1_EPT) + threadIdx.x;
-  for (int it = 0; it < MSG1_EPT; ++it) {
-    const int i = base + it*256;
-    if (i >= N_EDGES) break;
-    const int dst = dst_perm[i];
-    const int src = src_perm[i];
-    float acc[EMB];
-    const uint4* pd = (const uint4*)(pb + (size_t)dst*EMB);
-    const uint4* qs = (const uint4*)(qb + (size_t)src*EMB);
-#pragma unroll
-    for (int j4 = 0; j4 < 4; ++j4) {
-      const uint4 a = pd[j4];
-      const uint4 b = qs[j4];
-      const unsigned ua[4] = {a.x, a.y, a.z, a.w};
-      const unsigned ub[4] = {b.x, b.y, b.z, b.w};
-#pragma unroll
-      for (int t = 0; t < 4; ++t) {
-        acc[j4*8 + 2*t]   = bf2f((unsigned short)(ua[t] & 0xFFFFu)) +
-                            bf2f((unsigned short)(ub[t] & 0xFFFFu));
-        acc[j4*8 + 2*t+1] = bf2f((unsigned short)(ua[t] >> 16)) +
-                            bf2f((unsigned short)(ub[t] >> 16));
-      }
-    }
-    const uint4 eraw = *(const uint4*)(ea_perm + (size_t)i*ED);
-    const unsigned ue[4] = {eraw.x, eraw.y, eraw.z, eraw.w};
-    float ev[8];
-#pragma unroll
-    for (int t = 0; t < 4; ++t) {
-      ev[2*t]   = bf2f((unsigned short)(ue[t] & 0xFFFFu));
-      ev[2*t+1] = bf2f((unsigned short)(ue[t] >> 16));
-    }
-#pragma unroll
-    for (int k = 0; k < 8; ++k) {
-      const float* wk = w1b + k*EMB;
-#pragma unroll
-      for (int c = 0; c < EMB; ++c) acc[c] = fmaf(ev[k], wk[c], acc[c]);
-    }
-
-    unsigned short us[EMB];
-#pragma unroll
-    for (int c = 0; c < EMB; ++c) us[c] = f2bf(acc[c]);
-    unsigned u[16];
-#pragma unroll
-    for (int j = 0; j < 16; ++j)
-      u[j] = (unsigned)us[2*j] | ((unsigned)us[2*j+1] << 16);
-    uint4* dp = (uint4*)(y + (size_t)i*EMB);
-#pragma unroll
-    for (int j = 0; j < 4; ++j) {
-      uint4 o; o.x = u[4*j]; o.y = u[4*j+1]; o.z = u[4*j+2]; o.w = u[4*j+3];
-      dp[j] = o;
-    }
-#pragma unroll
-    for (int c = 0; c < EMB; ++c) {
-      const float v = bf2f(us[c]);
-      ts[c] += v;
-      tss[c] = fmaf(v, v, tss[c]);
-    }
-  }
-  block_stats_atomic(ts, tss, stats);
-}
-
-__global__ __launch_bounds__(256) void k_msg2(
-    unsigned short* __restrict__ y,
-    const float* __restrict__ stats1, const float* __restrict__ g1, const float* __restrict__ be1,
-    const float* __restrict__ w2, const float* __restrict__ b2,
-    float* __restrict__ stats2)
-{
-  __shared__ __align__(16) unsigned short lds_t[4][16*32];
-  __shared__ float lds_s[4][32], lds_q[4][32];
-  __shared__ float cf[64];
-
-  coef_from_stats(stats1, g1, be1, 1.0f/(float)N_EDGES, cf);
-
-  const int lane = threadIdx.x & 63;
-  const int wid  = threadIdx.x >> 6;
-  const int n0 = lane & 15;
-  const int kb = lane >> 4;
-
-  bf16x8 Blo, Bhi;
-#pragma unroll
-  for (int j = 0; j < 8; ++j) {
-    Blo[j] = (short)f2bf(w2[(kb*8 + j)*EMB + n0]);
-    Bhi[j] = (short)f2bf(w2[(kb*8 + j)*EMB + 16 + n0]);
-  }
-  float a1[8], c1[8];
-#pragma unroll
-  for (int j = 0; j < 8; ++j) {
-    a1[j] = cf[kb*8 + j];
-    c1[j] = cf[EMB + kb*8 + j];
-  }
-  const float b2c0 = b2[n0], b2c1 = b2[16 + n0];
-
-  float ts[8], tss[8];
-#pragma unroll
-  for (int j = 0; j < 8; ++j) { ts[j] = 0.f; tss[j] = 0.f; }
-
-  const int tile0 = blockIdx.x * (MSG2_TPW*4);
-  for (int t = 0; t < MSG2_TPW; ++t) {
-    const int tile = tile0 + t*4 + wid;
-    if (tile >= NT16) break;
-    const size_t e0 = (size_t)tile * 16;
-
-    const uint4 araw = *(const uint4*)(y + (e0 + n0)*EMB + kb*8);
-    unsigned int ua[4] = {araw.x, araw.y, araw.z, araw.w};
-    bf16x8 A;
-#pragma unroll
-    for (int j = 0; j < 4; ++j) {
-      float v0 = bf2f((unsigned short)(ua[j] & 0xFFFFu));
-      float v1 = bf2f((unsigned short)(ua[j] >> 16));
-      v0 = fmaxf(fmaf(a1[2*j],   v0, c1[2*j]),   0.f);
-      v1 = fmaxf(fmaf(a1[2*j+1], v1, c1[2*j+1]), 0.f);
-      A[2*j]   = (short)f2bf(v0);
-      A[2*j+1] = (short)f2bf(v1);
-    }
-
-    f32x4 acc0 = {0.f, 0.f, 0.f, 0.f};
-    f32x4 acc1 = {0.f, 0.f, 0.f, 0.f};
-    acc0 = __builtin_amdgcn_mfma_f32_16x16x32_bf16(A, Blo, acc0, 0, 0, 0);
-    acc1 = __builtin_amdgcn_mfma_f32_16x16x32_bf16(A, Bhi, acc1, 0, 0, 0);
-
-#pragma unroll
-    for (int r = 0; r < 4; ++r) {
-      const int row = kb*4 + r;
-      lds_t[wid][row*32 + n0]      = f2bf(acc0[r] + b2c0);
-      lds_t[wid][row*32 + 16 + n0] = f2bf(acc1[r] + b2c1);
-    }
-    const uint4 orow = *(const uint4*)&lds_t[wid][(lane>>2)*32 + (lane&3)*8];
-    *(uint4*)(y + (e0 + (lane>>2))*EMB + (lane&3)*8) = orow;
-
-    unsigned int uo[4] = {orow.x, orow.y, orow.z, orow.w};
-#pragma unroll
-    for (int j = 0; j < 4; ++j) {
-      const float v0 = bf2f((unsigned short)(uo[j] & 0xFFFFu));
-      const float v1 = bf2f((unsigned short)(uo[j] >> 16));
-      ts[2*j]   += v0;  tss[2*j]   = fmaf(v0, v0, tss[2*j]);
-      ts[2*j+1] += v1;  tss[2*j+1] = fmaf(v1, v1, tss[2*j+1]);
-    }
-  }
-
-#pragma unroll
-  for (int j = 0; j < 8; ++j) {
-    float s = ts[j], qq = tss[j];
-#pragma unroll
-    for (int o = 4; o < 64; o <<= 1) {
-      s  += __shfl_xor(s, o, 64);
-      qq += __shfl_xor(qq, o, 64);
-    }
-    ts[j] = s; tss[j] = qq;
-  }
-  if (lane < 4) {
-#pragma unroll
-    for (int j = 0; j < 8; ++j) {
-      lds_s[wid][lane*8 + j] = ts[j];
-      lds_q[wid][lane*8 + j] = tss[j];
-    }
-  }
-  __syncthreads();
-  if (threadIdx.x < 64) {
-    const int c = threadIdx.x & 31;
-    const int kind = threadIdx.x >> 5;
-    float v = 0.f;
-#pragma unroll
-    for (int wq = 0; wq < 4; ++wq)
-      v += kind ? lds_q[wq][c] : lds_s[wq][c];
-    atomicAdd(stats2 + ((blockIdx.x & (SREP-1)) << 6) + kind*32 + c, v);
-  }
-}
-
-__global__ __launch_bounds__(256) void k_aggr(
-    const unsigned short* __restrict__ y, const int* __restrict__ row_ptr,
-    const float* __restrict__ stats2, const float* __restrict__ g2, const float* __restrict__ be2,
-    float* __restrict__ aggr)
-{
-  __shared__ float cf[64];
-  coef_from_stats(stats2, g2, be2, 1.0f/(float)N_EDGES, cf);
-
-  const int grp = threadIdx.x >> 5;
-  const int l   = threadIdx.x & 31;
-  const int rof = l >> 4;
-  const int cp  = l & 15;
-  const int n = blockIdx.x*8 + grp;
-  if (n >= N_NODES) return;
-  const float a0 = cf[2*cp],     b0 = cf[EMB + 2*cp];
-  const float a1 = cf[2*cp + 1], b1 = cf[EMB + 2*cp + 1];
-  const int lo = row_ptr[n], hi = row_ptr[n+1];
-  float s0 = 0.f, s1 = 0.f;
-  for (int i = lo + rof; i < hi; i += 2) {
-    const unsigned u = *(const unsigned*)(y + (size_t)i*EMB + 2*cp);
-    const float v0 = bf2f((unsigned short)(u & 0xFFFFu));
-    const float v1 = bf2f((unsigned short)(u >> 16));
-    s0 += fmaxf(fmaf(a0, v0, b0), 0.f);
-    s1 += fmaxf(fmaf(a1, v1, b1), 0.f);
-  }
-  s0 += __shfl_xor(s0, 16, 64);
-  s1 += __shfl_xor(s1, 16, 64);
-  if (rof == 0) {
-    float2 o; o.x = s0; o.y = s1;
-    *(float2*)(aggr + (size_t)n*EMB + 2*cp) = o;
-  }
-}
-
-__global__ void k_pool(const float* __restrict__ h, const int* __restrict__ batch,
-                       const float* __restrict__ pw, const float* __restrict__ pb,
-                       float* __restrict__ out)
-{
-  __shared__ float sred[256];
-  __shared__ float hg[EMB];
-  const int b = blockIdx.x;
-  int lo = 0, hi = N_NODES;
-  while (lo < hi) { int m = (lo + hi) >> 1; if (batch[m] < b) lo = m + 1; else hi = m; }
-  const int start = lo;
-  hi = N_NODES;
-  while (lo < hi) { int m = (lo + hi) >> 1; if (batch[m] < b + 1) lo = m + 1; else hi = m; }
-  const int end = lo;
-
-  const int c = threadIdx.x & (EMB-1);
-  const int r = threadIdx.x >> 5;
-  float s = 0.f;
-  for (int n = start + r; n < end; n += 8) s += h[(size_t)n*EMB + c];
-  sred[threadIdx.x] = s;
-  __syncthreads();
-  if (threadIdx.x < EMB) {
-    float tot = 0.f;
-#pragma unroll
-    for (int r2 = 0; r2 < 8; ++r2) tot += sred[r2*EMB + threadIdx.x];
-    const float cnt = (float)(end - start);
-    hg[threadIdx.x] = tot / fmaxf(cnt, 1.f);
-  }
-  __syncthreads();
-  if (threadIdx.x < OUTD) {
-    float acc = pb[threadIdx.x];
-#pragma unroll
-    for (int cc = 0; cc < EMB; ++cc) acc = fmaf(hg[cc], pw[cc*OUTD + threadIdx.x], acc);
-    out[b*OUTD + threadIdx.x] = acc;
+
+  for (int b = blockIdx.x; b < NB; b += nblk) {
+    int lo = 0, hi = N_NODES;
+    while (lo < hi) { int m = (lo + hi) >> 1; if (a.batch[m] < b) lo = m + 1; else hi = m; }
+    const int start = lo;
+    hi = N_NODES;
+    while (lo < hi) { int m = (lo + hi) >> 1; if (a.batch[m] < b + 1) lo = m + 1; else hi = m; }
+    const int end = lo;
+
+    const int c = tid & (EMB-1);
+    const int r = tid >> 5;
+    float s = 0.f;
+    for (int n = start + r; n < end; n += 8) s += a.h[(size_t)n*EMB + c];
+    sred[tid] = s;
+    __syncthreads();
+    if (tid < EMB) {
+      float tot = 0.f;
+#pragma unroll
+      for (int r2 = 0; r2 < 8; ++r2) tot += sred[r2*EMB + tid];
+      const float cnt = (float)(end - start);
+      hg[tid] = tot / fmaxf(cnt, 1.f);
+    }
+    __syncthreads();
+    if (tid < OUTD) {
+      float acc = a.pred_b[tid];
+#pragma unroll
+      for (int cc = 0; cc < EMB; ++cc) acc = fmaf(hg[cc], a.pred_w[cc*OUTD + tid], acc);
+      a.out[b*OUTD + tid] = acc;
+    }
+    __syncthreads();
   }
 }
 
@@ -639,86 +636,59 @@
 extern "C" void kernel_launch(void* const* d_in, const int* in_sizes, int n_in,
                               void* d_out, int out_size, void* d_ws, size_t ws_size,
                               hipStream_t stream) {
-  const float* x        = (const float*)d_in[0];
-  const int*   ei       = (const int*)  d_in[1];
-  const float* ea       = (const float*)d_in[2];
-  const int*   batch    = (const int*)  d_in[3];
-  const float* lin_in_w = (const float*)d_in[4];
-  const float* lin_in_b = (const float*)d_in[5];
-  const float* msg_w1   = (const float*)d_in[6];
-  const float* msg_b1   = (const float*)d_in[7];
-  const float* msg_g1   = (const float*)d_in[8];
-  const float* msg_be1  = (const float*)d_in[9];
-  const float* msg_w2   = (const float*)d_in[10];
-  const float* msg_b2   = (const float*)d_in[11];
-  const float* msg_g2   = (const float*)d_in[12];
-  const float* msg_be2  = (const float*)d_in[13];
-  const float* upd_w1   = (const float*)d_in[14];
-  const float* upd_b1   = (const float*)d_in[15];
-  const float* upd_g1   = (const float*)d_in[16];
-  const float* upd_be1  = (const float*)d_in[17];
-  const float* upd_w2   = (const float*)d_in[18];
-  const float* upd_b2   = (const float*)d_in[19];
-  const float* upd_g2   = (const float*)d_in[20];
-  const float* upd_be2  = (const float*)d_in[21];
-  const float* pred_w   = (const float*)d_in[22];
-  const float* pred_b   = (const float*)d_in[23];
-  float* out = (float*)d_out;
+  KArgs a;
+  a.x        = (const float*)d_in[0];
+  a.ei       = (const int*)  d_in[1];
+  a.ea       = (const float*)d_in[2];
+  a.batch    = (const int*)  d_in[3];
+  a.lin_in_w = (const float*)d_in[4];
+  a.lin_in_b = (const float*)d_in[5];
+  a.msg_w1   = (const float*)d_in[6];
+  a.msg_b1   = (const float*)d_in[7];
+  a.msg_g1   = (const float*)d_in[8];
+  a.msg_be1  = (const float*)d_in[9];
+  a.msg_w2   = (const float*)d_in[10];
+  a.msg_b2   = (const float*)d_in[11];
+  a.msg_g2   = (const float*)d_in[12];
+  a.msg_be2  = (const float*)d_in[13];
+  a.upd_w1   = (const float*)d_in[14];
+  a.upd_b1   = (const float*)d_in[15];
+  a.upd_g1   = (const float*)d_in[16];
+  a.upd_be1  = (const float*)d_in[17];
+  a.upd_w2   = (const float*)d_in[18];
+  a.upd_b2   = (const float*)d_in[19];
+  a.upd_g2   = (const float*)d_in[20];
+  a.upd_be2  = (const float*)d_in[21];
+  a.pred_w   = (const float*)d_in[22];
+  a.pred_b   = (const float*)d_in[23];
+  a.out      = (float*)d_out;
 
   char* wsb = (char*)d_ws;
-  unsigned short* y  = (unsigned short*)wsb;
-  unsigned short* eap= (unsigned short*)(wsb + (size_t)N_EDGES*EMB*2);
-  unsigned short* p  = eap + (size_t)N_EDGES*ED;
-  unsigned short* q  = p + (size_t)N_NODES*EMB;
-  float* h       = (float*)(q + (size_t)N_NODES*EMB);
-  float* aggr    = h + (size_t)N_NODES*EMB;
-  float* stats   = aggr + (size_t)N_NODES*EMB;
-  int*   cnt     = (int*)(stats + 16*SREP*64);
-  int*   cnt2    = cnt + N_NODES;
-  int*   row_ptr = cnt2 + N_NODES;
-  int*   bsum    = row_ptr + N_NODES + 1;
-  int*   perm    = bsum + 256;
-  int*   src_perm= perm + N_EDGES;
-  int*   dst_perm= src_perm + N_EDGES;
-  const size_t need = ((size_t)((char*)(dst_perm + N_EDGES) - wsb));
+  a.y   = (unsigned short*)wsb;
+  a.eap = (unsigned short*)(wsb + (size_t)N_EDGES*EMB*2);
+  a.p   = a.eap + (size_t)N_EDGES*ED;
+  a.q   = a.p + (size_t)N_NODES*EMB;
+  a.h     = (float*)(a.q + (size_t)N_NODES*EMB);
+  a.aggr  = a.h + (size_t)N_NODES*EMB;
+  a.z     = a.aggr + (size_t)N_NODES*EMB;
+  a.stats = a.z + (size_t)N_NODES*EMB;
+  a.cnt     = (int*)(a.stats + 16*SREP*64);
+  a.cnt2    = a.cnt + N_NODES;
+  a.row_ptr = a.cnt2 + N_NODES;
+  a.bsum    = a.row_ptr + N_NODES + 1;
+  a.perm    = a.bsum + 256;
+  a.src_perm= a.perm + N_EDGES;
+  a.dst_perm= a.src_perm + N_EDGES;
+  const size_t need = ((size_t)((char*)(a.dst_perm + N_EDGES) - wsb));
   if (ws_size < need) return;
 
-  hipMemsetAsync(stats, 0, (16*SREP*64 + 2*N_NODES)*sizeof(float), stream);
-
-  k_lin_in_pq<<<NODE4_GRID, 256, 0, stream>>>(x, lin_in_w, lin_in_b, msg_w1, msg_b1, h, p, q);
-  k_hist<<<EDGE_GRID, 256, 0, stream>>>(ei, cnt);
-  k_scan_a<<<NODE_GRID, 256, 0, stream>>>(cnt, row_ptr, bsum);
-  k_scan_b<<<1, 256, 0, stream>>>(bsum, row_ptr);
-  k_scan_c<<<NODE_GRID, 256, 0, stream>>>(row_ptr, bsum);
-  k_place<<<EDGE_GRID, 256, 0, stream>>>(ei, row_ptr, cnt2, perm);
-  k_permute<<<EDGE_GRID, 256, 0, stream>>>(perm, ei, ea, src_perm, dst_perm, eap);
-
-  for (int l = 0; l < NLAYERS; ++l) {
-    const int st = l*4;
-    const float* w1  = msg_w1 + (size_t)l*(2*EMB+ED)*EMB;
-    const float* w1b = w1 + (size_t)2*EMB*EMB;
-    const float* w2  = msg_w2 + (size_t)l*EMB*EMB;
-    const float* uw1 = upd_w1 + (size_t)l*(2*EMB)*EMB;
-    const float* uw2 = upd_w2 + (size_t)l*EMB*EMB;
-    const float* w1_next = (l+1 < NLAYERS) ? msg_w1 + (size_t)(l+1)*(2*EMB+ED)*EMB : nullptr;
-    const float* b1_next = (l+1 < NLAYERS) ? msg_b1 + (size_t)(l+1)*EMB : nullptr;
-
-    k_msg1<<<MSG1_GRID, 256, 0, stream>>>(p, q, src_perm, dst_perm, eap,
-                                          w1b, y, stats + (size_t)st*SREP*64);
-    k_msg2<<<MSG2_GRID, 256, 0, stream>>>(y, stats + (size_t)st*SREP*64,
-                                          msg_g1 + l*EMB, msg_be1 + l*EMB,
-                                          w2, msg_b2 + l*EMB, stats + (size_t)(st+1)*SREP*64);
-    k_aggr<<<AGGR_GRID, 256, 0, stream>>>(y, row_ptr, stats + (size_t)(st+1)*SREP*64,
-                                          msg_g2 + l*EMB, msg_be2 + l*EMB, aggr);
-    k_upd1<<<NODE4_GRID, 256, 0, stream>>>(h, aggr, uw1, upd_b1 + l*EMB,
-                                           stats + (size_t)(st+2)*SREP*64);
-    k_upd2<<<NODE4_GRID, 256, 0, stream>>>(aggr, stats + (size_t)(st+2)*SREP*64,
-                                           upd_g1 + l*EMB, upd_be1 + l*EMB,
-                                           uw2, upd_b2 + l*EMB, stats + (size_t)(st+3)*SREP*64);
-    k_resid_pq<<<NODE4_GRID, 256, 0, stream>>>(h, aggr, stats + (size_t)(st+3)*SREP*64,
-                                               upd_g2 + l*EMB, upd_be2 + l*EMB,
-                                               w1_next, b1_next, p, q);
-  }
-
-  k_pool<<<NB, 256, 0, stream>>>(h, batch, pred_w, pred_b, out);
+  hipMemsetAsync(a.stats, 0, (16*SREP*64 + 2*N_NODES)*sizeof(float), stream);
+
+  int occ = 0;
+  hipOccupancyMaxActiveBlocksPerMultiprocessor(&occ, (const void*)k_all, 256, 0);
+  if (occ < 1) occ = 1;
+  int grid = occ * 256;
+  if (grid > 1024) grid = 1024;
+  void* kargs[] = { (void*)&a };
+  hipLaunchCooperativeKernel((const void*)k_all, dim3(grid), dim3(256), kargs, 0, stream);
 }
```

After: 2.932 ms. 208% more time.
